# Kernel optimization log

Measured on AMD Instinct MI355X. Metric: run time of the kernel, lower is better.

The kernel has to match this reference:

```python
import jax, jax.numpy as jnp
import numpy as np

TOPK = 32
NUM_PT = 8192
NUM_KP = 8
HW = 19200


def _conv3(x, w, b):
    # x: [1, C, N], w: [O, C, 3] -> [1, O, N] (padding=1)
    y = jax.lax.conv_general_dilated(x, w, (1,), [(1, 1)],
                                     dimension_numbers=('NCH', 'OIH', 'NCH'))
    return y + b[None, :, None]


def setup_inputs() -> dict:
    key = jax.random.key(0)
    ks = jax.random.split(key, 64)

    def p(i, *shape):
        return (jax.random.normal(ks[i], shape, dtype=jnp.float32) * 0.05)

    inp = {
        'seg': jax.random.uniform(ks[0], (1, NUM_PT), dtype=jnp.float32),
        'img': jax.random.normal(ks[1], (1, 32, HW), dtype=jnp.float32),
        'cloud': jax.random.normal(ks[2], (1, NUM_PT, 3), dtype=jnp.float32),
        't': jax.random.normal(ks[3], (1, 3), dtype=jnp.float32),
        'choose': jax.random.randint(ks[4], (1, 1, NUM_PT), 0, HW),
        # Pseudo3DConv params (all 1x1 conv1d == channel matmul)
        'pconv1_w': p(5, 64, 3),    'pconv1_b': p(6, 64),
        'pconv2_w': p(7, 128, 64),  'pconv2_b': p(8, 128),
        'conv1_w': p(9, 64, 32),    'conv1_b': p(10, 64),
        'conv2_w': p(11, 128, 64),  'conv2_b': p(12, 128),
        'psconv1_w': p(13, 256, 128), 'psconv1_b': p(14, 256),
        'psconv2_w': p(15, 128, 256), 'psconv2_b': p(16, 128),
        'final_w': p(17, 128, 416), 'final_b': p(18, 128),
        # heads
        'seg1_w': p(19, 64, 128, 3), 'seg1_b': p(20, 64),
        'seg2_w': p(21, 32, 64),     'seg2_b': p(22, 32),
        'seg3_w': p(23, 1, 32),      'seg3_b': p(24, 1),
        'dis1_w': p(25, 64, 128, 3), 'dis1_b': p(26, 64),
        'dis2_w': p(27, 32, 64),     'dis2_b': p(28, 32),
        'dis3_w': p(29, 1, 32),      'dis3_b': p(30, 1),
        'lin1_w': p(31, 90, 128),    'lin1_b': p(32, 90),
        'lin2_w': p(33, 64, 90),     'lin2_b': p(34, 64),
        'lin3_w': p(35, 3 * NUM_KP, 64), 'lin3_b': p(36, 3 * NUM_KP),
    }
    return inp


def reference(seg, img, cloud, t, choose,
              pconv1_w, pconv1_b, pconv2_w, pconv2_b,
              conv1_w, conv1_b, conv2_w, conv2_b,
              psconv1_w, psconv1_b, psconv2_w, psconv2_b,
              final_w, final_b,
              seg1_w, seg1_b, seg2_w, seg2_b, seg3_w, seg3_b,
              dis1_w, dis1_b, dis2_w, dis2_b, dis3_w, dis3_b,
              lin1_w, lin1_b, lin2_w, lin2_b, lin3_w, lin3_b):
    lrelu = jax.nn.leaky_relu  # slope 0.01, same as torch default
    N = NUM_PT

    # gather per-point image features at chosen pixels: [N, 32]
    feat = jnp.take(img[0], choose[0, 0], axis=1).T
    c = cloud[0]  # [N, 3]

    # ---- KNN (self included, as in knn_cuda) ----
    d2 = jnp.sum((c[:, None, :] - c[None, :, :]) ** 2, axis=-1)  # [N, N]
    _, idx = jax.lax.top_k(-d2, TOPK)  # [N, K] nearest neighbors

    # ---- point-feature MLP (pconv1 -> lrelu -> pconv2) ----
    pf = lrelu(c @ pconv1_w.T + pconv1_b) @ pconv2_w.T + pconv2_b  # [N, 128]

    # ---- vectorized per-point neighbor gather + MLP + weighted maxpool ----
    nf = feat[idx]    # [N, K, 32]
    npf = pf[idx]     # [N, K, 128]
    npos = c[idx]     # [N, K, 3]
    w = jax.nn.softmax(-jnp.linalg.norm(c[:, None, :] - npos, axis=-1), axis=1)  # [N, K]

    f = lrelu(nf @ conv1_w.T + conv1_b) @ conv2_w.T + conv2_b          # [N, K, 128]
    fp = lrelu(npf @ psconv1_w.T + psconv1_b) @ psconv2_w.T + psconv2_b  # [N, K, 128]
    f = jnp.max(f * w[..., None], axis=1)    # [N, 128]
    fp = jnp.max(fp * w[..., None], axis=1)  # [N, 128]

    # final2 = [fp | img_feat], final1 = [f | cloud_feat] -> cat -> [N, 416]
    final = jnp.concatenate([fp, feat, f, pf], axis=1)
    fused = lrelu(final) @ final_w.T + final_b  # [N, 128]
    fused = fused.T[None]  # [1, 128, N]

    def pw(x, w_, b_):  # 1x1 conv1d on [1, C, N]
        return jnp.einsum('oc,bcn->bon', w_, x) + b_[None, :, None]

    # segmentation head
    h = lrelu(_conv3(fused, seg1_w, seg1_b))
    seg_pre = pw(lrelu(pw(h, seg2_w, seg2_b)), seg3_w, seg3_b).reshape(1, N)

    # distance-to-center weighting (norm along coord dim, softmax over points)
    dis_center = jax.nn.softmax(
        jnp.linalg.norm(cloud - (-t)[:, None, :], axis=2), axis=1)  # [1, N]

    # distance head (on unweighted fused features, matching torch op order)
    h = lrelu(_conv3(fused, dis1_w, dis1_b))
    dis_pre = pw(lrelu(pw(h, dis2_w, dis2_b)), dis3_w, dis3_b).reshape(1, N)

    # weight fused features by center distance and segmentation, sum-pool
    fused = fused * dis_center[:, None, :] * seg[:, None, :]
    g = jnp.sum(fused, axis=2)  # [1, 128]

    kp = lrelu(g @ lin1_w.T + lin1_b)
    kp = lrelu(kp @ lin2_w.T + lin2_b)
    keypoints = (kp @ lin3_w.T + lin3_b).reshape(1, NUM_KP, 3)
    return keypoints, dis_pre, dis_center, seg_pre
```

## Files before the change

### kernel.cpp

```cpp
#include <hip/hip_runtime.h>
#include <math.h>

#define NPT 8192
#define HWIMG 19200
#define KCAP 128

using short8 = __attribute__((ext_vector_type(8))) short;
using short4v = __attribute__((ext_vector_type(4))) short;
using f32x4  = __attribute__((ext_vector_type(4))) float;

__device__ __forceinline__ float lrelu(float x) { return x > 0.f ? x : 0.01f * x; }
__device__ __forceinline__ unsigned short f2bf(float v) {
  unsigned u = __float_as_uint(v);
  return (unsigned short)((u + 0x7fffu + ((u >> 16) & 1u)) >> 16);
}
__device__ __forceinline__ float bf2f(unsigned short h) {
  return __uint_as_float(((unsigned)h) << 16);
}
__device__ __forceinline__ void split2(float v, unsigned short& h, unsigned short& l) {
  h = f2bf(v);
  l = f2bf(v - bf2f(h));
}
__device__ __forceinline__ void mfma3(f32x4& acc, short8 ah, short8 al, short8 wh, short8 wl) {
  acc = __builtin_amdgcn_mfma_f32_16x16x32_bf16(ah, wh, acc, 0, 0, 0);
  acc = __builtin_amdgcn_mfma_f32_16x16x32_bf16(al, wh, acc, 0, 0, 0);
  acc = __builtin_amdgcn_mfma_f32_16x16x32_bf16(ah, wl, acc, 0, 0, 0);
}

__device__ __forceinline__ int swz(int o, int k, int Kc) {
  return ((((o >> 4) * Kc + (k >> 5)) << 6) + (((k >> 3) & 3) << 4) + (o & 15)) * 8 + (k & 7);
}

#define OFF_PCONV2  0
#define OFF_CONV1   8192
#define OFF_CONV2   10240
#define OFF_PSCONV1 18432
#define OFF_PSCONV2 51200
#define OFF_FINAL   83968
#define OFF_W3      137216
#define OFF_W2P     186368

#define S_C4    NPT
#define S_G     129
#define S_BIASC 128
#define S_B2C   64
#define S_FEAT  (NPT*32)
#define S_W3    49152
#define S_W2P   8192
#define S_WSPL  OFF_W3
#define PREP_TOTAL (S_C4 + S_G + S_BIASC + S_B2C + S_FEAT + S_W3 + S_W2P + S_WSPL)
__global__ void k_prep(const float* __restrict__ cloud, const int* __restrict__ choose,
                       const float* __restrict__ img,
                       const float* __restrict__ seg1_w, const float* __restrict__ dis1_w,
                       const float* __restrict__ seg1_b, const float* __restrict__ dis1_b,
                       const float* __restrict__ seg2_w, const float* __restrict__ dis2_w,
                       const float* __restrict__ seg2_b, const float* __restrict__ dis2_b,
                       const float* __restrict__ pconv2_w, const float* __restrict__ conv1_w,
                       const float* __restrict__ conv2_w, const float* __restrict__ psconv1_w,
                       const float* __restrict__ psconv2_w, const float* __restrict__ final_w,
                       float* __restrict__ c4, float* __restrict__ g,
                       float* __restrict__ biasc, float* __restrict__ bias2c,
                       float* __restrict__ feat,
                       unsigned short* __restrict__ feat_h, unsigned short* __restrict__ feat_l,
                       unsigned short* __restrict__ Wh, unsigned short* __restrict__ Wl) {
  int j = blockIdx.x * blockDim.x + threadIdx.x;
  if (j < S_C4) {
    float x = cloud[j*3+0], y = cloud[j*3+1], z = cloud[j*3+2];
    float4 v; v.x = x; v.y = y; v.z = z; v.w = x*x + y*y + z*z;
    ((float4*)c4)[j] = v;
    return;
  }
  j -= S_C4;
  if (j < S_G) { g[j] = 0.f; return; }
  j -= S_G;
  if (j < S_BIASC) { biasc[j] = (j < 64) ? seg1_b[j] : dis1_b[j-64]; return; }
  j -= S_BIASC;
  if (j < S_B2C) { bias2c[j] = (j < 32) ? seg2_b[j] : dis2_b[j-32]; return; }
  j -= S_B2C;
  if (j < S_FEAT) {
    int n = j >> 5, ch = j & 31;
    float v = img[ch*HWIMG + choose[n]];
    feat[j] = v;
    unsigned short hh, ll; split2(v, hh, ll);
    int d = swz(n, ch, 1);
    feat_h[d] = hh; feat_l[d] = ll;
    return;
  }
  j -= S_FEAT;
  if (j < S_W3) {
    int h = j / 24576, r = j - h*24576, o = r / 384, k = r - o*384;
    int t = k >> 7, c = k & 127;
    float v = (h ? dis1_w : seg1_w)[o*384 + c*3 + t];
    unsigned short hh, ll; split2(v, hh, ll);
    int d = OFF_W3 + swz(h*64 + o, k, 12);
    Wh[d] = hh; Wl[d] = ll;
    return;
  }
  j -= S_W3;
  if (j < S_W2P) {
    int o = j >> 7, c = j & 127;
    float v = 0.f;
    if (o < 32) { if (c < 64) v = seg2_w[o*64 + c]; }
    else        { if (c >= 64) v = dis2_w[(o-32)*64 + (c-64)]; }
    unsigned short hh, ll; split2(v, hh, ll);
    int d = OFF_W2P + swz(o, c, 4);
    Wh[d] = hh; Wl[d] = ll;
    return;
  }
  j -= S_W2P;
  if (j < S_WSPL) {
    float v; int d;
    if (j < OFF_CONV1) {
      int o = j >> 6, k = j & 63;
      v = pconv2_w[j]; d = OFF_PCONV2 + swz(o, k, 2);
    } else if (j < OFF_CONV2) {
      int jj = j - OFF_CONV1, o = jj >> 5, k = jj & 31;
      v = conv1_w[jj]; d = OFF_CONV1 + swz(o, k, 1);
    } else if (j < OFF_PSCONV1) {
      int jj = j - OFF_CONV2, o = jj >> 6, k = jj & 63;
      v = conv2_w[jj]; d = OFF_CONV2 + swz(o, k, 2);
    } else if (j < OFF_PSCONV2) {
      int jj = j - OFF_PSCONV1, o = jj >> 7, k = jj & 127;
      v = psconv1_w[jj]; d = OFF_PSCONV1 + swz(o, k, 4);
    } else if (j < OFF_FINAL) {
      int jj = j - OFF_PSCONV2, o = jj >> 8, k = jj & 255;
      v = psconv2_w[jj]; d = OFF_PSCONV2 + swz(o, k, 8);
    } else {
      int jj = j - OFF_FINAL, o = jj / 416, k = jj - o*416;
      v = final_w[jj]; d = OFF_FINAL + swz(o, k, 13);
    }
    unsigned short hh, ll; split2(v, hh, ll);
    Wh[d] = hh; Wl[d] = ll;
  }
}

__device__ __forceinline__ unsigned bsort32u(unsigned key, int lane) {
#pragma unroll
  for (int k = 2; k <= 64; k <<= 1) {
#pragma unroll
    for (int j = k >> 1; j > 0; j >>= 1) {
      unsigned o = __shfl_xor(key, j, 64);
      bool keepmin = (((lane & j) == 0) == ((lane & k) == 0));
      key = ((o < key) == keepmin) ? o : key;
    }
  }
  return key;
}
__device__ __forceinline__ unsigned long long bsort64(unsigned long long key, int lane) {
#pragma unroll
  for (int k = 2; k <= 64; k <<= 1) {
#pragma unroll
    for (int j = k >> 1; j > 0; j >>= 1) {
      unsigned long long o = __shfl_xor(key, j, 64);
      bool keepmin = (((lane & j) == 0) == ((lane & k) == 0));
      bool omin = o < key;
      key = (omin == keepmin) ? o : key;
    }
  }
  return key;
}
__device__ __forceinline__ unsigned long long bmerge64(unsigned long long key, int lane) {
#pragma unroll
  for (int j = 32; j > 0; j >>= 1) {
    unsigned long long o = __shfl_xor(key, j, 64);
    bool keepmin = ((lane & j) == 0);
    bool omin = o < key;
    key = (omin == keepmin) ? o : key;
  }
  return key;
}

#define MEGA_GRID 3073
__global__ __launch_bounds__(256) void k_mega(const float4* __restrict__ c4,
                                              int* __restrict__ idxo, float* __restrict__ wo,
                                              const float* __restrict__ cloud,
                                              const float* __restrict__ tvec,
                                              float* __restrict__ dc,
                                              const float* __restrict__ pconv1_w, const float* __restrict__ pconv1_b,
                                              const float* __restrict__ pconv2_b, const float* __restrict__ psconv1_b,
                                              const float* __restrict__ psconv2_b,
                                              const unsigned short* __restrict__ feat_h,
                                              const unsigned short* __restrict__ feat_l,
                                              const float* __restrict__ conv1_b, const float* __restrict__ conv2_b,
                                              const unsigned short* __restrict__ Wh,
                                              const unsigned short* __restrict__ Wl,
                                              float* __restrict__ pf, float* __restrict__ Yfp,
                                              float* __restrict__ Yf) {
  __shared__ __align__(16) char smem[16384];
  int tid = threadIdx.x, lane = tid & 63, w = tid >> 6;
  int mr = lane & 15, q = lane >> 4;
  if (blockIdx.x > 2048) {
    unsigned short* sh_h = (unsigned short*)smem;
    unsigned short* sh_l = (unsigned short*)(smem + 8192);
    int cb = blockIdx.x - 2049;
    if (cb < 512) {
      int m0 = cb * 16;
      float4 cp = c4[m0 + mr];
      short8 ah0, al0, ah1, al1;
#pragma unroll
      for (int j = 0; j < 8; ++j) {
        int c0 = q*8 + j, c1 = 32 + q*8 + j;
        float v0 = lrelu(fmaf(cp.x, pconv1_w[c0*3+0], fmaf(cp.y, pconv1_w[c0*3+1],
                          fmaf(cp.z, pconv1_w[c0*3+2], pconv1_b[c0]))));
        float v1 = lrelu(fmaf(cp.x, pconv1_w[c1*3+0], fmaf(cp.y, pconv1_w[c1*3+1],
                          fmaf(cp.z, pconv1_w[c1*3+2], pconv1_b[c1]))));
        unsigned short hh, ll;
        split2(v0, hh, ll); ah0[j] = (short)hh; al0[j] = (short)ll;
        split2(v1, hh, ll); ah1[j] = (short)hh; al1[j] = (short)ll;
      }
      f32x4 acc[2];
#pragma unroll
      for (int t = 0; t < 2; ++t) { f32x4 z = {0.f,0.f,0.f,0.f}; acc[t] = z; }
      const unsigned short* W2h = Wh + OFF_PCONV2;
      const unsigned short* W2l = Wl + OFF_PCONV2;
#pragma unroll
      for (int tt = 0; tt < 2; ++tt) {
        int t1 = 2*w + tt;
        int w0 = ((t1*2 + 0)*64 + lane)*8, w1 = ((t1*2 + 1)*64 + lane)*8;
        mfma3(acc[tt], ah0, al0, *(const short8*)(W2h + w0), *(const short8*)(W2l + w0));
        mfma3(acc[tt], ah1, al1, *(const short8*)(W2h + w1), *(const short8*)(W2l + w1));
      }
#pragma unroll
      for (int tt = 0; tt < 2; ++tt) {
        int t1 = 2*w + tt, n = t1*16 + mr;
        float b = pconv2_b[n];
        int ks2 = t1 >> 1, q2 = (t1 & 1)*2 + (mr >> 3), jd = mr & 7;
#pragma unroll
        for (int r = 0; r < 4; ++r) {
          int row = q*4 + r;
          float v = acc[tt][r] + b;
          pf[(size_t)(m0+row)*128 + n] = v;
          unsigned short hh, ll; split2(v, hh, ll);
          int p = ((ks2*16 + row)*4 + q2)*8 + jd;
          sh_h[p] = hh; sh_l[p] = ll;
        }
      }
      __syncthreads();
      f32x4 acc3[2];
#pragma unroll
      for (int t = 0; t < 2; ++t) { f32x4 z = {0.f,0.f,0.f,0.f}; acc3[t] = z; }
      const unsigned short* W3h = Wh + OFF_PSCONV1;
      const unsigned short* W3l = Wl + OFF_PSCONV1;
      const unsigned short* W4h = Wh + OFF_PSCONV2;
      const unsigned short* W4l = Wl + OFF_PSCONV2;
#pragma unroll
      for (int h = 0; h < 2; ++h) {
        f32x4 acc2[2];
#pragma unroll
        for (int t = 0; t < 2; ++t) { f32x4 z = {0.f,0.f,0.f,0.f}; acc2[t] = z; }
#pragma unroll
        for (int ks = 0; ks < 4; ++ks) {
          int ap = ((ks*16 + mr)*4 + q)*8;
          short8 ah = *(const short8*)&sh_h[ap];
          short8 al = *(const short8*)&sh_l[ap];
#pragma unroll
          for (int tt = 0; tt < 2; ++tt) {
            int ts = h*8 + 2*w + tt;
            int wb = ((ts*4 + ks)*64 + lane)*8;
            mfma3(acc2[tt], ah, al, *(const short8*)(W3h + wb), *(const short8*)(W3l + wb));
          }
        }
#pragma unroll
        for (int tt = 0; tt < 2; ++tt) {
          int tl = 2*w + tt;
          int n = h*128 + tl*16 + mr;
          float b = psconv1_b[n];
          int ks3 = tl >> 1, q3 = (tl & 1)*2 + (mr >> 3), jd = mr & 7;
#pragma unroll
          for (int r = 0; r < 4; ++r) {
            int row = q*4 + r;
            float v = lrelu(acc2[tt][r] + b);
            unsigned short hh, ll; split2(v, hh, ll);
            int p = 2048 + ((ks3*16 + row)*4 + q3)*8 + jd;
            sh_h[p] = hh; sh_l[p] = ll;
          }
        }
        __syncthreads();
#pragma unroll
        for (int ks = 0; ks < 4; ++ks) {
          int ap = 2048 + ((ks*16 + mr)*4 + q)*8;
          short8 ah = *(const short8*)&sh_h[ap];
          short8 al = *(const short8*)&sh_l[ap];
#pragma unroll
          for (int tt = 0; tt < 2; ++tt) {
            int wb = (((2*w+tt)*8 + h*4 + ks)*64 + lane)*8;
            mfma3(acc3[tt], ah, al, *(const short8*)(W4h + wb), *(const short8*)(W4l + wb));
          }
        }
        __syncthreads();
      }
#pragma unroll
      for (int tt = 0; tt < 2; ++tt) {
        int n = (2*w+tt)*16 + mr;
        float b = psconv2_b[n];
#pragma unroll
        for (int r = 0; r < 4; ++r)
          Yfp[(size_t)(m0 + q*4 + r)*128 + n] = acc3[tt][r] + b;
      }
    } else {
      int m0 = (cb - 512) * 16;
      int ab = ((m0 >> 4)*64 + lane)*8;
      short8 ah = *(const short8*)(feat_h + ab);
      short8 al = *(const short8*)(feat_l + ab);
      f32x4 acc = {0.f,0.f,0.f,0.f};
      const unsigned short* W1h = Wh + OFF_CONV1;
      const unsigned short* W1l = Wl + OFF_CONV1;
      {
        int wb = (w*64 + lane)*8;
        mfma3(acc, ah, al, *(const short8*)(W1h + wb), *(const short8*)(W1l + wb));
      }
      {
        int n = w*16 + mr;
        float b = conv1_b[n];
        int ks2 = n >> 5, q2 = (n >> 3) & 3, jd = mr & 7;
#pragma unroll
        for (int r = 0; r < 4; ++r) {
          int row = q*4 + r;
          float v = lrelu(acc[r] + b);
          unsigned short hh, ll; split2(v, hh, ll);
          int p = ((ks2*16 + row)*4 + q2)*8 + jd;
          sh_h[p] = hh; sh_l[p] = ll;
        }
      }
      __syncthreads();
      f32x4 acc2[2];
#pragma unroll
      for (int t = 0; t < 2; ++t) { f32x4 z = {0.f,0.f,0.f,0.f}; acc2[t] = z; }
      const unsigned short* W2h = Wh + OFF_CONV2;
      const unsigned short* W2l = Wl + OFF_CONV2;
#pragma unroll
      for (int ks = 0; ks < 2; ++ks) {
        int ap = ((ks*16 + mr)*4 + q)*8;
        short8 a2 = *(const short8*)&sh_h[ap];
        short8 a2l = *(const short8*)&sh_l[ap];
#pragma unroll
        for (int tt = 0; tt < 2; ++tt) {
          int wb = (((2*w+tt)*2 + ks)*64 + lane)*8;
          mfma3(acc2[tt], a2, a2l, *(const short8*)(W2h + wb), *(const short8*)(W2l + wb));
        }
      }
#pragma unroll
      for (int tt = 0; tt < 2; ++tt) {
        int n = (2*w+tt)*16 + mr;
        float b = conv2_b[n];
#pragma unroll
        for (int r = 0; r < 4; ++r)
          Yf[(size_t)(m0 + q*4 + r)*128 + n] = acc2[tt][r] + b;
      }
    }
    return;
  }
  if (blockIdx.x == 2048) {
    float* sred = (float*)smem;
    float tx = tvec[0], ty = tvec[1], tz = tvec[2];
    float v[32];
    float m = -INFINITY;
#pragma unroll
    for (int i2 = 0; i2 < 32; ++i2) {
      int n = i2*256 + tid;
      float ax = cloud[n*3+0] + tx, ay = cloud[n*3+1] + ty, az = cloud[n*3+2] + tz;
      v[i2] = sqrtf(ax*ax + ay*ay + az*az);
      m = fmaxf(m, v[i2]);
    }
#pragma unroll
    for (int o = 1; o < 64; o <<= 1) m = fmaxf(m, __shfl_xor(m, o, 64));
    if (lane == 0) sred[w] = m;
    __syncthreads();
    m = fmaxf(fmaxf(sred[0], sred[1]), fmaxf(sred[2], sred[3]));
    __syncthreads();
    float s = 0.f;
#pragma unroll
    for (int i2 = 0; i2 < 32; ++i2) { v[i2] = expf(v[i2] - m); s += v[i2]; }
#pragma unroll
    for (int o = 1; o < 64; o <<= 1) s += __shfl_xor(s, o, 64);
    if (lane == 0) sred[w] = s;
    __syncthreads();
    s = sred[0] + sred[1] + sred[2] + sred[3];
#pragma unroll
    for (int i2 = 0; i2 < 32; ++i2) dc[i2*256 + tid] = v[i2] / s;
    return;
  }
  float (*smin)[256] = (float(*)[256])smem;
  float* sTv = (float*)(smem + 4096);
  int*   scnt = (int*)(smem + 4112);
  float (*sd)[KCAP] = (float(*)[KCAP])(smem + 4128);
  int   (*sj)[KCAP] = (int(*)[KCAP])(smem + 6176);
  int q0 = blockIdx.x * 4;
  float4 p0 = c4[q0], p1 = c4[q0+1], p2 = c4[q0+2], p3 = c4[q0+3];
  float p0x = -2.f*p0.x, p0y = -2.f*p0.y, p0z = -2.f*p0.z;
  float p1x = -2.f*p1.x, p1y = -2.f*p1.y, p1z = -2.f*p1.z;
  float p2x = -2.f*p2.x, p2y = -2.f*p2.y, p2z = -2.f*p2.z;
  float p3x = -2.f*p3.x, p3y = -2.f*p3.y, p3z = -2.f*p3.z;
#define DDOT(PX,PY,PZ,PW,CJ) fmaf(PX,(CJ).x, fmaf(PY,(CJ).y, fmaf(PZ,(CJ).z, PW + (CJ).w)))
  float m0 = INFINITY, m1 = INFINITY, m2 = INFINITY, m3 = INFINITY;
  for (int t = 0; t < 32; ++t) {
    float4 cj = c4[t*256 + tid];
    m0 = fminf(m0, DDOT(p0x,p0y,p0z,p0.w,cj));
    m1 = fminf(m1, DDOT(p1x,p1y,p1z,p1.w,cj));
    m2 = fminf(m2, DDOT(p2x,p2y,p2z,p2.w,cj));
    m3 = fminf(m3, DDOT(p3x,p3y,p3z,p3.w,cj));
  }
  smin[0][tid] = m0; smin[1][tid] = m1; smin[2][tid] = m2; smin[3][tid] = m3;
  if (tid < 4) scnt[tid] = 0;
  __syncthreads();
  {
    float4 vv = *(const float4*)&smin[w][lane*4];
    float m4 = fmaxf(fminf(fminf(vv.x, vv.y), fminf(vv.z, vv.w)), 0.f);
    unsigned key = bsort32u(__float_as_uint(m4), lane);
    float T = __uint_as_float(__shfl(key, 31, 64));
    if (lane == 0) sTv[w] = T * (1.f + 2e-5f) + 4e-5f;
  }
  __syncthreads();
  float T0 = sTv[0], T1 = sTv[1], T2 = sTv[2], T3 = sTv[3];
  for (int t = 0; t < 32; ++t) {
    int j = t*256 + tid;
    float4 cj = c4[j];
    float d;
#define APPEND(Q, P) { \
    float dx_ = (P).x-cj.x, dy_ = (P).y-cj.y, dz_ = (P).z-cj.z; \
    float de_ = dx_*dx_ + dy_*dy_ + dz_*dz_; \
    int p_ = atomicAdd(&scnt[Q],1); if (p_ < KCAP) { sd[Q][p_] = de_; sj[Q][p_] = j; } }
    d = DDOT(p0x,p0y,p0z,p0.w,cj); if (d <= T0) APPEND(0, p0);
    d = DDOT(p1x,p1y,p1z,p1.w,cj); if (d <= T1) APPEND(1, p1);
    d = DDOT(p2x,p2y,p2z,p2.w,cj); if (d <= T2) APPEND(2, p2);
    d = DDOT(p3x,p3y,p3z,p3.w,cj); if (d <= T3) APPEND(3, p3);
  }
  __syncthreads();
  int M = scnt[w]; if (M > KCAP) M = KCAP;
  unsigned long long key = (lane < M)
      ? (((unsigned long long)__float_as_uint(sd[w][lane]) << 32) | (unsigned)sj[w][lane])
      : ~0ull;
  key = bsort64(key, lane);
  for (int base = 64; base < M; base += 64) {
    unsigned long long nk = (base + lane < M)
        ? (((unsigned long long)__float_as_uint(sd[w][base+lane]) << 32) | (unsigned)sj[w][base+lane])
        : ~0ull;
    nk = bsort64(nk, lane);
    nk = __shfl_xor(nk, 63, 64);
    key = key < nk ? key : nk;
    key = bmerge64(key, lane);
  }
  float dsel = __uint_as_float((unsigned)(key >> 32));
  int   jsel = (int)(unsigned)(key & 0xffffffffu);
  float v = -sqrtf(dsel);
  float mx = v;
#pragma unroll
  for (int o = 1; o < 32; o <<= 1) mx = fmaxf(mx, __shfl_xor(mx, o, 64));
  float e = expf(v - mx);
  float s = e;
#pragma unroll
  for (int o = 1; o < 32; o <<= 1) s += __shfl_xor(s, o, 64);
  if (lane < 32) {
    int qd = q0 + w;
    wo[qd*32 + lane] = e / s;
    idxo[qd*32 + lane] = jsel;
  }
}

__global__ __launch_bounds__(256) void k_tail(const float* __restrict__ Yf,
                                              const float* __restrict__ Yfp,
                                              const float* __restrict__ feat,
                                              const float* __restrict__ pf,
                                              const int* __restrict__ idx,
                                              const float* __restrict__ wsm,
                                              const unsigned short* __restrict__ Wh,
                                              const unsigned short* __restrict__ Wl,
                                              const float* __restrict__ final_b,
                                              const float* __restrict__ biasc,
                                              const float* __restrict__ bias2c,
                                              const float* __restrict__ segw, const float* __restrict__ segb,
                                              const float* __restrict__ disw, const float* __restrict__ disb,
                                              unsigned short* __restrict__ fusedh,
                                              unsigned short* __restrict__ fusedl,
                                              float* __restrict__ osegp, float* __restrict__ odisp) {
  __shared__ int sjn[18][32];
  __shared__ float swn[18][32];
  __shared__ __align__(16) char sbuf[37440];
  int tid = threadIdx.x, lane = tid & 63, w = tid >> 6;
  int mr = lane & 15, q = lane >> 4;
  int mt = blockIdx.x, m0 = mt * 16;
  for (int t = tid; t < 18*32; t += 256) {
    int lr = t >> 5, k = t & 31, gr = m0 - 1 + lr;
    if (gr >= 0 && gr < NPT) { sjn[lr][k] = idx[gr*32+k]; swn[lr][k] = wsm[gr*32+k]; }
    else { sjn[lr][k] = 0; swn[lr][k] = 0.f; }
  }
  __syncthreads();
  for (int t = tid; t < 1872; t += 256) {
    int lr, col;
    float4 v4;
    if (t < 1152) {
      lr = t >> 6; int arr = (t >> 5) & 1, cg = t & 31;
      const float* Y = arr ? Yf : Yfp;
      float ax = -INFINITY, ay = -INFINITY, az = -INFINITY, aw = -INFINITY;
#pragma unroll 8
      for (int k = 0; k < 32; ++k) {
        float4 vv = *(const float4*)&Y[(size_t)sjn[lr][k]*128 + cg*4];
        float wk = swn[lr][k];
        ax = fmaxf(ax, wk*vv.x); ay = fmaxf(ay, wk*vv.y);
        az = fmaxf(az, wk*vv.z); aw = fmaxf(aw, wk*vv.w);
      }
      v4.x = lrelu(ax); v4.y = lrelu(ay); v4.z = lrelu(az); v4.w = lrelu(aw);
      col = (arr ? 160 : 0) + cg*4;
    } else if (t < 1728) {
      int u = t - 1152; lr = u >> 5; int cg = u & 31;
      int gr = m0 - 1 + lr;
      int gc = gr < 0 ? 0 : (gr >= NPT ? NPT-1 : gr);
      float4 p4 = *(const float4*)&pf[(size_t)gc*128 + cg*4];
      v4.x = lrelu(p4.x); v4.y = lrelu(p4.y); v4.z = lrelu(p4.z); v4.w = lrelu(p4.w);
      col = 288 + cg*4;
    } else {
      int u = t - 1728; lr = u >> 3; int cg = u & 7;
      int gr = m0 - 1 + lr;
      int gc = gr < 0 ? 0 : (gr >= NPT ? NPT-1 : gr);
      float4 p4 = *(const float4*)&feat[(size_t)gc*32 + cg*4];
      v4.x = lrelu(p4.x); v4.y = lrelu(p4.y); v4.z = lrelu(p4.z); v4.w = lrelu(p4.w);
      col = 128 + cg*4;
    }
    int gr = m0 - 1 + lr;
    if (gr < 0 || gr >= NPT) { v4.x = 0.f; v4.y = 0.f; v4.z = 0.f; v4.w = 0.f; }
    int ks = col >> 5, qq = (col >> 3) & 3, j0 = col & 7;
    char* base = sbuf + (ks*18 + lr)*80 + qq*16 + j0*2;
    short4v hv, lv;
    unsigned short hh, ll;
    split2(v4.x, hh, ll); hv[0] = (short)hh; lv[0] = (short)ll;
    split2(v4.y, hh, ll); hv[1] = (short)hh; lv[1] = (short)ll;
    split2(v4.z, hh, ll); hv[2] = (short)hh; lv[2] = (short)ll;
    split2(v4.w, hh, ll); hv[3] = (short)hh; lv[3] = (short)ll;
    *(short4v*)base = hv;
    *(short4v*)(base + 18720) = lv;
  }
  __syncthreads();
  f32x4 accA[2], accB[2];
#pragma unroll
  for (int t = 0; t < 2; ++t) {
    f32x4 z = {0.f,0.f,0.f,0.f}; accA[t] = z; accB[t] = z;
  }
  const unsigned short* WFh = Wh + OFF_FINAL;
  const unsigned short* WFl = Wl + OFF_FINAL;
#pragma unroll
  for (int ks = 0; ks < 13; ++ks) {
    int arB = 16 + mr; if (arB > 17) arB = 17;
    const char* pA = sbuf + (ks*18 + mr)*80 + q*16;
    const char* pB = sbuf + (ks*18 + arB)*80 + q*16;
    short8 ahA = *(const short8*)pA;
    short8 alA = *(const short8*)(pA + 18720);
    short8 ahB = *(const short8*)pB;
    short8 alB = *(const short8*)(pB + 18720);
#pragma unroll
    for (int tt = 0; tt < 2; ++tt) {
      int wb = (((2*w+tt)*13 + ks)*64 + lane)*8;
      short8 wh = *(const short8*)(WFh + wb);
      short8 wl = *(const short8*)(WFl + wb);
      mfma3(accA[tt], ahA, alA, wh, wl);
      mfma3(accB[tt], ahB, alB, wh, wl);
    }
  }
  __syncthreads();
#pragma unroll
  for (int tile = 0; tile < 2; ++tile) {
#pragma unroll
    for (int tt = 0; tt < 2; ++tt) {
      int t2 = 2*w + tt, n = t2*16 + mr;
      float b = final_b[n];
      int ksA = t2 >> 1, qq = (t2 & 1)*2 + (mr >> 3), jd = mr & 7;
#pragma unroll
      for (int r = 0; r < 4; ++r) {
        int lr = tile*16 + q*4 + r;
        if (lr > 17) continue;
        int gr = m0 - 1 + lr;
        float v = (tile ? accB[tt][r] : accA[tt][r]) + b;
        if (gr < 0 || gr >= NPT) v = 0.f;
        unsigned short hh, ll; split2(v, hh, ll);
        char* p = sbuf + (ksA*18 + lr)*80 + qq*16 + jd*2;
        *(unsigned short*)p = hh;
        *(unsigned short*)(p + 5760) = ll;
      }
    }
  }
  __syncthreads();
  {
    int ks2 = tid >> 6, q2 = (tid >> 4) & 3, mr2 = tid & 15;
    int lr = mr2 + 1;
    const char* p = sbuf + (ks2*18 + lr)*80 + q2*16;
    short8 oh = *(const short8*)p;
    short8 ol = *(const short8*)(p + 5760);
    size_t pos = ((size_t)mt*256 + tid)*8;
    *(short8*)(fusedh + pos) = oh;
    *(short8*)(fusedl + pos) = ol;
  }
  f32x4 acc3[2];
#pragma unroll
  for (int t = 0; t < 2; ++t) { f32x4 z = {0.f,0.f,0.f,0.f}; acc3[t] = z; }
  const unsigned short* W3h = Wh + OFF_W3;
  const unsigned short* W3l = Wl + OFF_W3;
#pragma unroll
  for (int ks = 0; ks < 12; ++ks) {
    int tap = ks >> 2, ksA = ks & 3;
    int ar = mr + tap;
    const char* p = sbuf + (ksA*18 + ar)*80 + q*16;
    short8 ah = *(const short8*)p;
    short8 al = *(const short8*)(p + 5760);
#pragma unroll
    for (int tt = 0; tt < 2; ++tt) {
      int wb = (((2*w+tt)*12 + ks)*64 + lane)*8;
      mfma3(acc3[tt], ah, al, *(const short8*)(W3h + wb), *(const short8*)(W3l + wb));
    }
  }
#pragma unroll
  for (int tt = 0; tt < 2; ++tt) {
    int t2 = 2*w + tt, n = t2*16 + mr;
    float b = biasc[n];
    int ks2 = t2 >> 1, q2 = (t2 & 1)*2 + (mr >> 3), jd = mr & 7;
#pragma unroll
    for (int r = 0; r < 4; ++r) {
      int row = q*4 + r;
      float v = lrelu(acc3[tt][r] + b);
      unsigned short hh, ll; split2(v, hh, ll);
      char* p = sbuf + 11520 + (ks2*16 + row)*80 + q2*16 + jd*2;
      *(unsigned short*)p = hh;
      *(unsigned short*)(p + 5120) = ll;
    }
  }
  __syncthreads();
  f32x4 acc4 = {0.f,0.f,0.f,0.f};
  const unsigned short* WPh = Wh + OFF_W2P;
  const unsigned short* WPl = Wl + OFF_W2P;
#pragma unroll
  for (int ks = 0; ks < 4; ++ks) {
    const char* p = sbuf + 11520 + (ks*16 + mr)*80 + q*16;
    short8 ah = *(const short8*)p;
    short8 al = *(const short8*)(p + 5120);
    int wb = ((w*4 + ks)*64 + lane)*8;
    mfma3(acc4, ah, al, *(const short8*)(WPh + wb), *(const short8*)(WPl + wb));
  }
  float hw = (w < 2) ? segw[w*16 + mr] : disw[(w-2)*16 + mr];
  float bb = bias2c[w*16 + mr];
  float* shead = (float*)(sbuf + 21760);
#pragma unroll
  for (int r = 0; r < 4; ++r)
    shead[(w*16 + q*4 + r)*17 + mr] = lrelu(acc4[r] + bb) * hw;
  __syncthreads();
  if (tid < 16) {
    float a = 0.f;
#pragma unroll
    for (int i = 0; i < 16; ++i) a += shead[(tid)*17 + i] + shead[(16 + tid)*17 + i];
    osegp[m0 + tid] = a + segb[0];
  } else if (tid < 32) {
    int r2 = tid - 16;
    float a = 0.f;
#pragma unroll
    for (int i = 0; i < 16; ++i) a += shead[(32 + r2)*17 + i] + shead[(48 + r2)*17 + i];
    odisp[m0 + r2] = a + disb[0];
  }
}

__global__ __launch_bounds__(256) void k_gk(const unsigned short* __restrict__ Ah,
                                            const unsigned short* __restrict__ Al,
                                            const float* __restrict__ dc,
                                            const float* __restrict__ seg,
                                            float* __restrict__ g,
                                            const float* __restrict__ l1w, const float* __restrict__ l1b,
                                            const float* __restrict__ l2w, const float* __restrict__ l2b,
                                            const float* __restrict__ l3w, const float* __restrict__ l3b,
                                            float* __restrict__ o_kp) {
  __shared__ float sred[2048];
  __shared__ int slast;
  int tid = threadIdx.x;
  int b = blockIdx.x;
  float pg[8] = {0.f,0.f,0.f,0.f,0.f,0.f,0.f,0.f};
  int mrr = tid & 15;
  for (int mi = 0; mi < 16; ++mi) {
    int m = b*16 + mi;
    int row = m*16 + mrr;
    float wrow = dc[row] * seg[row];
    size_t pos = ((size_t)m*256 + tid)*8;
    short8 hv = *(const short8*)(Ah + pos);
    short8 lv = *(const short8*)(Al + pos);
#pragma unroll
    for (int j = 0; j < 8; ++j)
      pg[j] += (bf2f((unsigned short)hv[j]) + bf2f((unsigned short)lv[j])) * wrow;
  }
#pragma unroll
  for (int j = 0; j < 8; ++j) sred[tid*8 + j] = pg[j];
  __syncthreads();
  if (tid < 128) {
    int ks = tid >> 5, q2 = (tid >> 3) & 3, j = tid & 7;
    float s = 0.f;
#pragma unroll
    for (int mr2 = 0; mr2 < 16; ++mr2) s += sred[((ks<<6) + (q2<<4) + mr2)*8 + j];
    atomicAdd(&g[tid], s);
  }
  __threadfence();
  __syncthreads();
  if (tid == 0) slast = (atomicAdd((int*)(g + 128), 1) == 31);
  __syncthreads();
  if (!slast) return;
  __shared__ float sg[128], s1[90], s2[64];
  if (tid < 128) sg[tid] = atomicAdd(&g[tid], 0.f);
  __syncthreads();
  if (tid < 90) {
    float a = l1b[tid];
    for (int i = 0; i < 128; ++i) a += sg[i]*l1w[tid*128+i];
    s1[tid] = lrelu(a);
  }
  __syncthreads();
  if (tid < 64) {
    float a = l2b[tid];
    for (int i = 0; i < 90; ++i) a += s1[i]*l2w[tid*90+i];
    s2[tid] = lrelu(a);
  }
  __syncthreads();
  if (tid < 24) {
    float a = l3b[tid];
    for (int i = 0; i < 64; ++i) a += s2[i]*l3w[tid*64+i];
    o_kp[tid] = a;
  }
}

extern "C" void kernel_launch(void* const* d_in, const int* in_sizes, int n_in,
                              void* d_out, int out_size, void* d_ws, size_t ws_size,
                              hipStream_t stream) {
  const float* seg      = (const float*)d_in[0];
  const float* img      = (const float*)d_in[1];
  const float* cloud    = (const float*)d_in[2];
  const float* tvec     = (const float*)d_in[3];
  const int*   choose   = (const int*)d_in[4];
  const float* pconv1_w = (const float*)d_in[5];
  const float* pconv1_b = (const float*)d_in[6];
  const float* pconv2_w = (const float*)d_in[7];
  const float* pconv2_b = (const float*)d_in[8];
  const float* conv1_w  = (const float*)d_in[9];
  const float* conv1_b  = (const float*)d_in[10];
  const float* conv2_w  = (const float*)d_in[11];
  const float* conv2_b  = (const float*)d_in[12];
  const float* psconv1_w= (const float*)d_in[13];
  const float* psconv1_b= (const float*)d_in[14];
  const float* psconv2_w= (const float*)d_in[15];
  const float* psconv2_b= (const float*)d_in[16];
  const float* final_w  = (const float*)d_in[17];
  const float* final_b  = (const float*)d_in[18];
  const float* seg1_w   = (const float*)d_in[19];
  const float* seg1_b   = (const float*)d_in[20];
  const float* seg2_w   = (const float*)d_in[21];
  const float* seg2_b   = (const float*)d_in[22];
  const float* seg3_w   = (const float*)d_in[23];
  const float* seg3_b   = (const float*)d_in[24];
  const float* dis1_w   = (const float*)d_in[25];
  const float* dis1_b   = (const float*)d_in[26];
  const float* dis2_w   = (const float*)d_in[27];
  const float* dis2_b   = (const float*)d_in[28];
  const float* dis3_w   = (const float*)d_in[29];
  const float* dis3_b   = (const float*)d_in[30];
  const float* lin1_w   = (const float*)d_in[31];
  const float* lin1_b   = (const float*)d_in[32];
  const float* lin2_w   = (const float*)d_in[33];
  const float* lin2_b   = (const float*)d_in[34];
  const float* lin3_w   = (const float*)d_in[35];
  const float* lin3_b   = (const float*)d_in[36];

  float* out = (float*)d_out;
  float* ws  = (float*)d_ws;

  float* c4     = ws + 0;
  float* feat   = ws + 32768;
  unsigned short* feat_h = (unsigned short*)(ws + 294912);
  unsigned short* feat_l = (unsigned short*)(ws + 425984);
  float* pf     = ws + 557056;
  float* Yf     = ws + 1605632;
  float* Yfp    = ws + 2654208;
  int*   idx    = (int*)(ws + 3702784);
  float* wsm    = ws + 3964928;
  unsigned short* fusedh = (unsigned short*)(ws + 8683520);
  unsigned short* fusedl = (unsigned short*)(ws + 9207808);
  unsigned short* Wh    = (unsigned short*)(ws + 9732096);
  unsigned short* Wl    = (unsigned short*)(ws + 9829376);
  float* biasc  = ws + 9926656;
  float* bias2c = ws + 9926784;
  float* g      = ws + 9926848;

  float* o_kp   = out;
  float* o_disp = out + 24;
  float* o_dc   = out + 8216;
  float* o_segp = out + 16408;

  k_prep<<<(PREP_TOTAL + 255)/256, 256, 0, stream>>>(
      cloud, choose, img, seg1_w, dis1_w, seg1_b, dis1_b,
      seg2_w, dis2_w, seg2_b, dis2_b,
      pconv2_w, conv1_w, conv2_w, psconv1_w, psconv2_w, final_w,
      c4, g, biasc, bias2c, feat, feat_h, feat_l, Wh, Wl);

  k_mega<<<MEGA_GRID, 256, 0, stream>>>(
      (const float4*)c4, idx, wsm, cloud, tvec, o_dc,
      pconv1_w, pconv1_b, pconv2_b, psconv1_b, psconv2_b,
      feat_h, feat_l, conv1_b, conv2_b, Wh, Wl, pf, Yfp, Yf);

  k_tail<<<512, 256, 0, stream>>>(
      Yf, Yfp, feat, pf, idx, wsm, Wh, Wl,
      final_b, biasc, bias2c, seg3_w, seg3_b, dis3_w, dis3_b,
      fusedh, fusedl, o_segp, o_disp);

  k_gk<<<32, 256, 0, stream>>>(fusedh, fusedl, o_dc, seg, g,
                               lin1_w, lin1_b, lin2_w, lin2_b, lin3_w, lin3_b, o_kp);

  (void)in_sizes; (void)n_in; (void)out_size; (void)ws_size;
}
```

Before: 230.0 us.

## Fuse all four kernels into one persistent cooperative kernel with grid syncs

Merges the prep, mega (knn/chain/softmax), tail and global-keypoint kernels into a single cooperative kernel. Blocks loop over virtual block indices, and grid.sync() separates the phases. This removes three kernel launches and their inter-kernel gaps. In exchange, the grid is capped by occupancy at up to 1024 blocks, so persistent blocks serialize work that used to be spread over thousands of blocks. Shared memory is now sized for the largest phase, which may limit occupancy, and each grid barrier has its own cost.

```diff
diff --git a/kernel.cpp b/kernel.cpp
--- a/kernel.cpp
+++ b/kernel.cpp
@@ -1,5 +1,8 @@
 #include <hip/hip_runtime.h>
+#include <hip/hip_cooperative_groups.h>
 #include <math.h>
+
+namespace cg = cooperative_groups;
 
 #define NPT 8192
 #define HWIMG 19200
@@ -26,7 +29,6 @@
   acc = __builtin_amdgcn_mfma_f32_16x16x32_bf16(al, wh, acc, 0, 0, 0);
   acc = __builtin_amdgcn_mfma_f32_16x16x32_bf16(ah, wl, acc, 0, 0, 0);
 }
-
 __device__ __forceinline__ int swz(int o, int k, int Kc) {
   return ((((o >> 4) * Kc + (k >> 5)) << 6) + (((k >> 3) & 3) << 4) + (o & 15)) * 8 + (k & 7);
 }
@@ -49,62 +51,101 @@
 #define S_W2P   8192
 #define S_WSPL  OFF_W3
 #define PREP_TOTAL (S_C4 + S_G + S_BIASC + S_B2C + S_FEAT + S_W3 + S_W2P + S_WSPL)
-__global__ void k_prep(const float* __restrict__ cloud, const int* __restrict__ choose,
-                       const float* __restrict__ img,
-                       const float* __restrict__ seg1_w, const float* __restrict__ dis1_w,
-                       const float* __restrict__ seg1_b, const float* __restrict__ dis1_b,
-                       const float* __restrict__ seg2_w, const float* __restrict__ dis2_w,
-                       const float* __restrict__ seg2_b, const float* __restrict__ dis2_b,
-                       const float* __restrict__ pconv2_w, const float* __restrict__ conv1_w,
-                       const float* __restrict__ conv2_w, const float* __restrict__ psconv1_w,
-                       const float* __restrict__ psconv2_w, const float* __restrict__ final_w,
-                       float* __restrict__ c4, float* __restrict__ g,
-                       float* __restrict__ biasc, float* __restrict__ bias2c,
-                       float* __restrict__ feat,
-                       unsigned short* __restrict__ feat_h, unsigned short* __restrict__ feat_l,
-                       unsigned short* __restrict__ Wh, unsigned short* __restrict__ Wl) {
-  int j = blockIdx.x * blockDim.x + threadIdx.x;
+
+struct Args {
+  const float *seg, *img, *cloud, *tvec;
+  const int* choose;
+  const float *pconv1_w, *pconv1_b, *pconv2_w, *pconv2_b;
+  const float *conv1_w, *conv1_b, *conv2_w, *conv2_b;
+  const float *psconv1_w, *psconv1_b, *psconv2_w, *psconv2_b;
+  const float *final_w, *final_b;
+  const float *seg1_w, *seg1_b, *seg2_w, *seg2_b, *seg3_w, *seg3_b;
+  const float *dis1_w, *dis1_b, *dis2_w, *dis2_b, *dis3_w, *dis3_b;
+  const float *lin1_w, *lin1_b, *lin2_w, *lin2_b, *lin3_w, *lin3_b;
+  float *c4, *g, *biasc, *bias2c, *feat, *pf, *Yf, *Yfp, *wsm;
+  int* idx;
+  unsigned short *feat_h, *feat_l, *fusedh, *fusedl, *Wh, *Wl;
+  float *o_kp, *o_disp, *o_dc, *o_segp;
+};
+
+__device__ __forceinline__ unsigned bsort32u(unsigned key, int lane) {
+#pragma unroll
+  for (int k = 2; k <= 64; k <<= 1) {
+#pragma unroll
+    for (int j = k >> 1; j > 0; j >>= 1) {
+      unsigned o = __shfl_xor(key, j, 64);
+      bool keepmin = (((lane & j) == 0) == ((lane & k) == 0));
+      key = ((o < key) == keepmin) ? o : key;
+    }
+  }
+  return key;
+}
+__device__ __forceinline__ unsigned long long bsort64(unsigned long long key, int lane) {
+#pragma unroll
+  for (int k = 2; k <= 64; k <<= 1) {
+#pragma unroll
+    for (int j = k >> 1; j > 0; j >>= 1) {
+      unsigned long long o = __shfl_xor(key, j, 64);
+      bool keepmin = (((lane & j) == 0) == ((lane & k) == 0));
+      bool omin = o < key;
+      key = (omin == keepmin) ? o : key;
+    }
+  }
+  return key;
+}
+__device__ __forceinline__ unsigned long long bmerge64(unsigned long long key, int lane) {
+#pragma unroll
+  for (int j = 32; j > 0; j >>= 1) {
+    unsigned long long o = __shfl_xor(key, j, 64);
+    bool keepmin = ((lane & j) == 0);
+    bool omin = o < key;
+    key = (omin == keepmin) ? o : key;
+  }
+  return key;
+}
+
+__device__ void prep_item(const Args& a, int j) {
   if (j < S_C4) {
-    float x = cloud[j*3+0], y = cloud[j*3+1], z = cloud[j*3+2];
+    float x = a.cloud[j*3+0], y = a.cloud[j*3+1], z = a.cloud[j*3+2];
     float4 v; v.x = x; v.y = y; v.z = z; v.w = x*x + y*y + z*z;
-    ((float4*)c4)[j] = v;
+    ((float4*)a.c4)[j] = v;
     return;
   }
   j -= S_C4;
-  if (j < S_G) { g[j] = 0.f; return; }
+  if (j < S_G) { a.g[j] = 0.f; return; }
   j -= S_G;
-  if (j < S_BIASC) { biasc[j] = (j < 64) ? seg1_b[j] : dis1_b[j-64]; return; }
+  if (j < S_BIASC) { a.biasc[j] = (j < 64) ? a.seg1_b[j] : a.dis1_b[j-64]; return; }
   j -= S_BIASC;
-  if (j < S_B2C) { bias2c[j] = (j < 32) ? seg2_b[j] : dis2_b[j-32]; return; }
+  if (j < S_B2C) { a.bias2c[j] = (j < 32) ? a.seg2_b[j] : a.dis2_b[j-32]; return; }
   j -= S_B2C;
   if (j < S_FEAT) {
     int n = j >> 5, ch = j & 31;
-    float v = img[ch*HWIMG + choose[n]];
-    feat[j] = v;
+    float v = a.img[ch*HWIMG + a.choose[n]];
+    a.feat[j] = v;
     unsigned short hh, ll; split2(v, hh, ll);
     int d = swz(n, ch, 1);
-    feat_h[d] = hh; feat_l[d] = ll;
+    a.feat_h[d] = hh; a.feat_l[d] = ll;
     return;
   }
   j -= S_FEAT;
   if (j < S_W3) {
     int h = j / 24576, r = j - h*24576, o = r / 384, k = r - o*384;
     int t = k >> 7, c = k & 127;
-    float v = (h ? dis1_w : seg1_w)[o*384 + c*3 + t];
+    float v = (h ? a.dis1_w : a.seg1_w)[o*384 + c*3 + t];
     unsigned short hh, ll; split2(v, hh, ll);
     int d = OFF_W3 + swz(h*64 + o, k, 12);
-    Wh[d] = hh; Wl[d] = ll;
+    a.Wh[d] = hh; a.Wl[d] = ll;
     return;
   }
   j -= S_W3;
   if (j < S_W2P) {
     int o = j >> 7, c = j & 127;
     float v = 0.f;
-    if (o < 32) { if (c < 64) v = seg2_w[o*64 + c]; }
-    else        { if (c >= 64) v = dis2_w[(o-32)*64 + (c-64)]; }
+    if (o < 32) { if (c < 64) v = a.seg2_w[o*64 + c]; }
+    else        { if (c >= 64) v = a.dis2_w[(o-32)*64 + (c-64)]; }
     unsigned short hh, ll; split2(v, hh, ll);
     int d = OFF_W2P + swz(o, c, 4);
-    Wh[d] = hh; Wl[d] = ll;
+    a.Wh[d] = hh; a.Wl[d] = ll;
     return;
   }
   j -= S_W2P;
@@ -112,280 +153,68 @@
     float v; int d;
     if (j < OFF_CONV1) {
       int o = j >> 6, k = j & 63;
-      v = pconv2_w[j]; d = OFF_PCONV2 + swz(o, k, 2);
+      v = a.pconv2_w[j]; d = OFF_PCONV2 + swz(o, k, 2);
     } else if (j < OFF_CONV2) {
       int jj = j - OFF_CONV1, o = jj >> 5, k = jj & 31;
-      v = conv1_w[jj]; d = OFF_CONV1 + swz(o, k, 1);
+      v = a.conv1_w[jj]; d = OFF_CONV1 + swz(o, k, 1);
     } else if (j < OFF_PSCONV1) {
       int jj = j - OFF_CONV2, o = jj >> 6, k = jj & 63;
-      v = conv2_w[jj]; d = OFF_CONV2 + swz(o, k, 2);
+      v = a.conv2_w[jj]; d = OFF_CONV2 + swz(o, k, 2);
     } else if (j < OFF_PSCONV2) {
       int jj = j - OFF_PSCONV1, o = jj >> 7, k = jj & 127;
-      v = psconv1_w[jj]; d = OFF_PSCONV1 + swz(o, k, 4);
+      v = a.psconv1_w[jj]; d = OFF_PSCONV1 + swz(o, k, 4);
     } else if (j < OFF_FINAL) {
       int jj = j - OFF_PSCONV2, o = jj >> 8, k = jj & 255;
-      v = psconv2_w[jj]; d = OFF_PSCONV2 + swz(o, k, 8);
+      v = a.psconv2_w[jj]; d = OFF_PSCONV2 + swz(o, k, 8);
     } else {
       int jj = j - OFF_FINAL, o = jj / 416, k = jj - o*416;
-      v = final_w[jj]; d = OFF_FINAL + swz(o, k, 13);
+      v = a.final_w[jj]; d = OFF_FINAL + swz(o, k, 13);
     }
     unsigned short hh, ll; split2(v, hh, ll);
-    Wh[d] = hh; Wl[d] = ll;
-  }
-}
-
-__device__ __forceinline__ unsigned bsort32u(unsigned key, int lane) {
-#pragma unroll
-  for (int k = 2; k <= 64; k <<= 1) {
-#pragma unroll
-    for (int j = k >> 1; j > 0; j >>= 1) {
-      unsigned o = __shfl_xor(key, j, 64);
-      bool keepmin = (((lane & j) == 0) == ((lane & k) == 0));
-      key = ((o < key) == keepmin) ? o : key;
-    }
-  }
-  return key;
-}
-__device__ __forceinline__ unsigned long long bsort64(unsigned long long key, int lane) {
-#pragma unroll
-  for (int k = 2; k <= 64; k <<= 1) {
-#pragma unroll
-    for (int j = k >> 1; j > 0; j >>= 1) {
-      unsigned long long o = __shfl_xor(key, j, 64);
-      bool keepmin = (((lane & j) == 0) == ((lane & k) == 0));
-      bool omin = o < key;
-      key = (omin == keepmin) ? o : key;
-    }
-  }
-  return key;
-}
-__device__ __forceinline__ unsigned long long bmerge64(unsigned long long key, int lane) {
-#pragma unroll
-  for (int j = 32; j > 0; j >>= 1) {
-    unsigned long long o = __shfl_xor(key, j, 64);
-    bool keepmin = ((lane & j) == 0);
-    bool omin = o < key;
-    key = (omin == keepmin) ? o : key;
-  }
-  return key;
-}
-
-#define MEGA_GRID 3073
-__global__ __launch_bounds__(256) void k_mega(const float4* __restrict__ c4,
-                                              int* __restrict__ idxo, float* __restrict__ wo,
-                                              const float* __restrict__ cloud,
-                                              const float* __restrict__ tvec,
-                                              float* __restrict__ dc,
-                                              const float* __restrict__ pconv1_w, const float* __restrict__ pconv1_b,
-                                              const float* __restrict__ pconv2_b, const float* __restrict__ psconv1_b,
-                                              const float* __restrict__ psconv2_b,
-                                              const unsigned short* __restrict__ feat_h,
-                                              const unsigned short* __restrict__ feat_l,
-                                              const float* __restrict__ conv1_b, const float* __restrict__ conv2_b,
-                                              const unsigned short* __restrict__ Wh,
-                                              const unsigned short* __restrict__ Wl,
-                                              float* __restrict__ pf, float* __restrict__ Yfp,
-                                              float* __restrict__ Yf) {
-  __shared__ __align__(16) char smem[16384];
-  int tid = threadIdx.x, lane = tid & 63, w = tid >> 6;
-  int mr = lane & 15, q = lane >> 4;
-  if (blockIdx.x > 2048) {
-    unsigned short* sh_h = (unsigned short*)smem;
-    unsigned short* sh_l = (unsigned short*)(smem + 8192);
-    int cb = blockIdx.x - 2049;
-    if (cb < 512) {
-      int m0 = cb * 16;
-      float4 cp = c4[m0 + mr];
-      short8 ah0, al0, ah1, al1;
-#pragma unroll
-      for (int j = 0; j < 8; ++j) {
-        int c0 = q*8 + j, c1 = 32 + q*8 + j;
-        float v0 = lrelu(fmaf(cp.x, pconv1_w[c0*3+0], fmaf(cp.y, pconv1_w[c0*3+1],
-                          fmaf(cp.z, pconv1_w[c0*3+2], pconv1_b[c0]))));
-        float v1 = lrelu(fmaf(cp.x, pconv1_w[c1*3+0], fmaf(cp.y, pconv1_w[c1*3+1],
-                          fmaf(cp.z, pconv1_w[c1*3+2], pconv1_b[c1]))));
-        unsigned short hh, ll;
-        split2(v0, hh, ll); ah0[j] = (short)hh; al0[j] = (short)ll;
-        split2(v1, hh, ll); ah1[j] = (short)hh; al1[j] = (short)ll;
-      }
-      f32x4 acc[2];
-#pragma unroll
-      for (int t = 0; t < 2; ++t) { f32x4 z = {0.f,0.f,0.f,0.f}; acc[t] = z; }
-      const unsigned short* W2h = Wh + OFF_PCONV2;
-      const unsigned short* W2l = Wl + OFF_PCONV2;
-#pragma unroll
-      for (int tt = 0; tt < 2; ++tt) {
-        int t1 = 2*w + tt;
-        int w0 = ((t1*2 + 0)*64 + lane)*8, w1 = ((t1*2 + 1)*64 + lane)*8;
-        mfma3(acc[tt], ah0, al0, *(const short8*)(W2h + w0), *(const short8*)(W2l + w0));
-        mfma3(acc[tt], ah1, al1, *(const short8*)(W2h + w1), *(const short8*)(W2l + w1));
-      }
-#pragma unroll
-      for (int tt = 0; tt < 2; ++tt) {
-        int t1 = 2*w + tt, n = t1*16 + mr;
-        float b = pconv2_b[n];
-        int ks2 = t1 >> 1, q2 = (t1 & 1)*2 + (mr >> 3), jd = mr & 7;
-#pragma unroll
-        for (int r = 0; r < 4; ++r) {
-          int row = q*4 + r;
-          float v = acc[tt][r] + b;
-          pf[(size_t)(m0+row)*128 + n] = v;
-          unsigned short hh, ll; split2(v, hh, ll);
-          int p = ((ks2*16 + row)*4 + q2)*8 + jd;
-          sh_h[p] = hh; sh_l[p] = ll;
-        }
-      }
-      __syncthreads();
-      f32x4 acc3[2];
-#pragma unroll
-      for (int t = 0; t < 2; ++t) { f32x4 z = {0.f,0.f,0.f,0.f}; acc3[t] = z; }
-      const unsigned short* W3h = Wh + OFF_PSCONV1;
-      const unsigned short* W3l = Wl + OFF_PSCONV1;
-      const unsigned short* W4h = Wh + OFF_PSCONV2;
-      const unsigned short* W4l = Wl + OFF_PSCONV2;
-#pragma unroll
-      for (int h = 0; h < 2; ++h) {
-        f32x4 acc2[2];
-#pragma unroll
-        for (int t = 0; t < 2; ++t) { f32x4 z = {0.f,0.f,0.f,0.f}; acc2[t] = z; }
-#pragma unroll
-        for (int ks = 0; ks < 4; ++ks) {
-          int ap = ((ks*16 + mr)*4 + q)*8;
-          short8 ah = *(const short8*)&sh_h[ap];
-          short8 al = *(const short8*)&sh_l[ap];
-#pragma unroll
-          for (int tt = 0; tt < 2; ++tt) {
-            int ts = h*8 + 2*w + tt;
-            int wb = ((ts*4 + ks)*64 + lane)*8;
-            mfma3(acc2[tt], ah, al, *(const short8*)(W3h + wb), *(const short8*)(W3l + wb));
-          }
-        }
-#pragma unroll
-        for (int tt = 0; tt < 2; ++tt) {
-          int tl = 2*w + tt;
-          int n = h*128 + tl*16 + mr;
-          float b = psconv1_b[n];
-          int ks3 = tl >> 1, q3 = (tl & 1)*2 + (mr >> 3), jd = mr & 7;
-#pragma unroll
-          for (int r = 0; r < 4; ++r) {
-            int row = q*4 + r;
-            float v = lrelu(acc2[tt][r] + b);
-            unsigned short hh, ll; split2(v, hh, ll);
-            int p = 2048 + ((ks3*16 + row)*4 + q3)*8 + jd;
-            sh_h[p] = hh; sh_l[p] = ll;
-          }
-        }
-        __syncthreads();
-#pragma unroll
-        for (int ks = 0; ks < 4; ++ks) {
-          int ap = 2048 + ((ks*16 + mr)*4 + q)*8;
-          short8 ah = *(const short8*)&sh_h[ap];
-          short8 al = *(const short8*)&sh_l[ap];
-#pragma unroll
-          for (int tt = 0; tt < 2; ++tt) {
-            int wb = (((2*w+tt)*8 + h*4 + ks)*64 + lane)*8;
-            mfma3(acc3[tt], ah, al, *(const short8*)(W4h + wb), *(const short8*)(W4l + wb));
-          }
-        }
-        __syncthreads();
-      }
-#pragma unroll
-      for (int tt = 0; tt < 2; ++tt) {
-        int n = (2*w+tt)*16 + mr;
-        float b = psconv2_b[n];
-#pragma unroll
-        for (int r = 0; r < 4; ++r)
-          Yfp[(size_t)(m0 + q*4 + r)*128 + n] = acc3[tt][r] + b;
-      }
-    } else {
-      int m0 = (cb - 512) * 16;
-      int ab = ((m0 >> 4)*64 + lane)*8;
-      short8 ah = *(const short8*)(feat_h + ab);
-      short8 al = *(const short8*)(feat_l + ab);
-      f32x4 acc = {0.f,0.f,0.f,0.f};
-      const unsigned short* W1h = Wh + OFF_CONV1;
-      const unsigned short* W1l = Wl + OFF_CONV1;
-      {
-        int wb = (w*64 + lane)*8;
-        mfma3(acc, ah, al, *(const short8*)(W1h + wb), *(const short8*)(W1l + wb));
-      }
-      {
-        int n = w*16 + mr;
-        float b = conv1_b[n];
-        int ks2 = n >> 5, q2 = (n >> 3) & 3, jd = mr & 7;
-#pragma unroll
-        for (int r = 0; r < 4; ++r) {
-          int row = q*4 + r;
-          float v = lrelu(acc[r] + b);
-          unsigned short hh, ll; split2(v, hh, ll);
-          int p = ((ks2*16 + row)*4 + q2)*8 + jd;
-          sh_h[p] = hh; sh_l[p] = ll;
-        }
-      }
-      __syncthreads();
-      f32x4 acc2[2];
-#pragma unroll
-      for (int t = 0; t < 2; ++t) { f32x4 z = {0.f,0.f,0.f,0.f}; acc2[t] = z; }
-      const unsigned short* W2h = Wh + OFF_CONV2;
-      const unsigned short* W2l = Wl + OFF_CONV2;
-#pragma unroll
-      for (int ks = 0; ks < 2; ++ks) {
-        int ap = ((ks*16 + mr)*4 + q)*8;
-        short8 a2 = *(const short8*)&sh_h[ap];
-        short8 a2l = *(const short8*)&sh_l[ap];
-#pragma unroll
-        for (int tt = 0; tt < 2; ++tt) {
-          int wb = (((2*w+tt)*2 + ks)*64 + lane)*8;
-          mfma3(acc2[tt], a2, a2l, *(const short8*)(W2h + wb), *(const short8*)(W2l + wb));
-        }
-      }
-#pragma unroll
-      for (int tt = 0; tt < 2; ++tt) {
-        int n = (2*w+tt)*16 + mr;
-        float b = conv2_b[n];
-#pragma unroll
-        for (int r = 0; r < 4; ++r)
-          Yf[(size_t)(m0 + q*4 + r)*128 + n] = acc2[tt][r] + b;
-      }
-    }
-    return;
-  }
-  if (blockIdx.x == 2048) {
-    float* sred = (float*)smem;
-    float tx = tvec[0], ty = tvec[1], tz = tvec[2];
-    float v[32];
-    float m = -INFINITY;
-#pragma unroll
-    for (int i2 = 0; i2 < 32; ++i2) {
-      int n = i2*256 + tid;
-      float ax = cloud[n*3+0] + tx, ay = cloud[n*3+1] + ty, az = cloud[n*3+2] + tz;
-      v[i2] = sqrtf(ax*ax + ay*ay + az*az);
-      m = fmaxf(m, v[i2]);
-    }
-#pragma unroll
-    for (int o = 1; o < 64; o <<= 1) m = fmaxf(m, __shfl_xor(m, o, 64));
-    if (lane == 0) sred[w] = m;
-    __syncthreads();
-    m = fmaxf(fmaxf(sred[0], sred[1]), fmaxf(sred[2], sred[3]));
-    __syncthreads();
-    float s = 0.f;
-#pragma unroll
-    for (int i2 = 0; i2 < 32; ++i2) { v[i2] = expf(v[i2] - m); s += v[i2]; }
-#pragma unroll
-    for (int o = 1; o < 64; o <<= 1) s += __shfl_xor(s, o, 64);
-    if (lane == 0) sred[w] = s;
-    __syncthreads();
-    s = sred[0] + sred[1] + sred[2] + sred[3];
-#pragma unroll
-    for (int i2 = 0; i2 < 32; ++i2) dc[i2*256 + tid] = v[i2] / s;
-    return;
-  }
+    a.Wh[d] = hh; a.Wl[d] = ll;
+  }
+}
+
+__device__ void dc_body(const Args& a, char* smem, int tid) {
+  float* sred = (float*)smem;
+  int lane = tid & 63, w = tid >> 6;
+  float tx = a.tvec[0], ty = a.tvec[1], tz = a.tvec[2];
+  float v[32];
+  float m = -INFINITY;
+#pragma unroll
+  for (int i2 = 0; i2 < 32; ++i2) {
+    int n = i2*256 + tid;
+    float ax = a.cloud[n*3+0] + tx, ay = a.cloud[n*3+1] + ty, az = a.cloud[n*3+2] + tz;
+    v[i2] = sqrtf(ax*ax + ay*ay + az*az);
+    m = fmaxf(m, v[i2]);
+  }
+#pragma unroll
+  for (int o = 1; o < 64; o <<= 1) m = fmaxf(m, __shfl_xor(m, o, 64));
+  if (lane == 0) sred[w] = m;
+  __syncthreads();
+  m = fmaxf(fmaxf(sred[0], sred[1]), fmaxf(sred[2], sred[3]));
+  __syncthreads();
+  float s = 0.f;
+#pragma unroll
+  for (int i2 = 0; i2 < 32; ++i2) { v[i2] = expf(v[i2] - m); s += v[i2]; }
+#pragma unroll
+  for (int o = 1; o < 64; o <<= 1) s += __shfl_xor(s, o, 64);
+  if (lane == 0) sred[w] = s;
+  __syncthreads();
+  s = sred[0] + sred[1] + sred[2] + sred[3];
+#pragma unroll
+  for (int i2 = 0; i2 < 32; ++i2) a.o_dc[i2*256 + tid] = v[i2] / s;
+}
+
+__device__ void knn_body(const Args& a, char* smem, int qb, int tid) {
   float (*smin)[256] = (float(*)[256])smem;
   float* sTv = (float*)(smem + 4096);
   int*   scnt = (int*)(smem + 4112);
   float (*sd)[KCAP] = (float(*)[KCAP])(smem + 4128);
   int   (*sj)[KCAP] = (int(*)[KCAP])(smem + 6176);
-  int q0 = blockIdx.x * 4;
+  int lane = tid & 63, w = tid >> 6;
+  const float4* c4 = (const float4*)a.c4;
+  int q0 = qb * 4;
   float4 p0 = c4[q0], p1 = c4[q0+1], p2 = c4[q0+2], p3 = c4[q0+3];
   float p0x = -2.f*p0.x, p0y = -2.f*p0.y, p0z = -2.f*p0.z;
   float p1x = -2.f*p1.x, p1y = -2.f*p1.y, p1z = -2.f*p1.z;
@@ -452,37 +281,185 @@
   for (int o = 1; o < 32; o <<= 1) s += __shfl_xor(s, o, 64);
   if (lane < 32) {
     int qd = q0 + w;
-    wo[qd*32 + lane] = e / s;
-    idxo[qd*32 + lane] = jsel;
-  }
-}
-
-__global__ __launch_bounds__(256) void k_tail(const float* __restrict__ Yf,
-                                              const float* __restrict__ Yfp,
-                                              const float* __restrict__ feat,
-                                              const float* __restrict__ pf,
-                                              const int* __restrict__ idx,
-                                              const float* __restrict__ wsm,
-                                              const unsigned short* __restrict__ Wh,
-                                              const unsigned short* __restrict__ Wl,
-                                              const float* __restrict__ final_b,
-                                              const float* __restrict__ biasc,
-                                              const float* __restrict__ bias2c,
-                                              const float* __restrict__ segw, const float* __restrict__ segb,
-                                              const float* __restrict__ disw, const float* __restrict__ disb,
-                                              unsigned short* __restrict__ fusedh,
-                                              unsigned short* __restrict__ fusedl,
-                                              float* __restrict__ osegp, float* __restrict__ odisp) {
-  __shared__ int sjn[18][32];
-  __shared__ float swn[18][32];
-  __shared__ __align__(16) char sbuf[37440];
-  int tid = threadIdx.x, lane = tid & 63, w = tid >> 6;
+    a.wsm[qd*32 + lane] = e / s;
+    a.idx[qd*32 + lane] = jsel;
+  }
+}
+
+__device__ void chain_body(const Args& a, char* smem, int cb, int tid) {
+  unsigned short* sh_h = (unsigned short*)smem;
+  unsigned short* sh_l = (unsigned short*)(smem + 8192);
+  int lane = tid & 63, w = tid >> 6;
   int mr = lane & 15, q = lane >> 4;
-  int mt = blockIdx.x, m0 = mt * 16;
+  const float4* c4 = (const float4*)a.c4;
+  if (cb < 512) {
+    int m0 = cb * 16;
+    float4 cp = c4[m0 + mr];
+    short8 ah0, al0, ah1, al1;
+#pragma unroll
+    for (int j = 0; j < 8; ++j) {
+      int c0 = q*8 + j, c1 = 32 + q*8 + j;
+      float v0 = lrelu(fmaf(cp.x, a.pconv1_w[c0*3+0], fmaf(cp.y, a.pconv1_w[c0*3+1],
+                        fmaf(cp.z, a.pconv1_w[c0*3+2], a.pconv1_b[c0]))));
+      float v1 = lrelu(fmaf(cp.x, a.pconv1_w[c1*3+0], fmaf(cp.y, a.pconv1_w[c1*3+1],
+                        fmaf(cp.z, a.pconv1_w[c1*3+2], a.pconv1_b[c1]))));
+      unsigned short hh, ll;
+      split2(v0, hh, ll); ah0[j] = (short)hh; al0[j] = (short)ll;
+      split2(v1, hh, ll); ah1[j] = (short)hh; al1[j] = (short)ll;
+    }
+    f32x4 acc[2];
+#pragma unroll
+    for (int t = 0; t < 2; ++t) { f32x4 z = {0.f,0.f,0.f,0.f}; acc[t] = z; }
+    const unsigned short* W2h = a.Wh + OFF_PCONV2;
+    const unsigned short* W2l = a.Wl + OFF_PCONV2;
+#pragma unroll
+    for (int tt = 0; tt < 2; ++tt) {
+      int t1 = 2*w + tt;
+      int w0 = ((t1*2 + 0)*64 + lane)*8, w1 = ((t1*2 + 1)*64 + lane)*8;
+      mfma3(acc[tt], ah0, al0, *(const short8*)(W2h + w0), *(const short8*)(W2l + w0));
+      mfma3(acc[tt], ah1, al1, *(const short8*)(W2h + w1), *(const short8*)(W2l + w1));
+    }
+#pragma unroll
+    for (int tt = 0; tt < 2; ++tt) {
+      int t1 = 2*w + tt, n = t1*16 + mr;
+      float b = a.pconv2_b[n];
+      int ks2 = t1 >> 1, q2 = (t1 & 1)*2 + (mr >> 3), jd = mr & 7;
+#pragma unroll
+      for (int r = 0; r < 4; ++r) {
+        int row = q*4 + r;
+        float v = acc[tt][r] + b;
+        a.pf[(size_t)(m0+row)*128 + n] = v;
+        unsigned short hh, ll; split2(v, hh, ll);
+        int p = ((ks2*16 + row)*4 + q2)*8 + jd;
+        sh_h[p] = hh; sh_l[p] = ll;
+      }
+    }
+    __syncthreads();
+    f32x4 acc3[2];
+#pragma unroll
+    for (int t = 0; t < 2; ++t) { f32x4 z = {0.f,0.f,0.f,0.f}; acc3[t] = z; }
+    const unsigned short* W3h = a.Wh + OFF_PSCONV1;
+    const unsigned short* W3l = a.Wl + OFF_PSCONV1;
+    const unsigned short* W4h = a.Wh + OFF_PSCONV2;
+    const unsigned short* W4l = a.Wl + OFF_PSCONV2;
+#pragma unroll
+    for (int h = 0; h < 2; ++h) {
+      f32x4 acc2[2];
+#pragma unroll
+      for (int t = 0; t < 2; ++t) { f32x4 z = {0.f,0.f,0.f,0.f}; acc2[t] = z; }
+#pragma unroll
+      for (int ks = 0; ks < 4; ++ks) {
+        int ap = ((ks*16 + mr)*4 + q)*8;
+        short8 ah = *(const short8*)&sh_h[ap];
+        short8 al = *(const short8*)&sh_l[ap];
+#pragma unroll
+        for (int tt = 0; tt < 2; ++tt) {
+          int ts = h*8 + 2*w + tt;
+          int wb = ((ts*4 + ks)*64 + lane)*8;
+          mfma3(acc2[tt], ah, al, *(const short8*)(W3h + wb), *(const short8*)(W3l + wb));
+        }
+      }
+#pragma unroll
+      for (int tt = 0; tt < 2; ++tt) {
+        int tl = 2*w + tt;
+        int n = h*128 + tl*16 + mr;
+        float b = a.psconv1_b[n];
+        int ks3 = tl >> 1, q3 = (tl & 1)*2 + (mr >> 3), jd = mr & 7;
+#pragma unroll
+        for (int r = 0; r < 4; ++r) {
+          int row = q*4 + r;
+          float v = lrelu(acc2[tt][r] + b);
+          unsigned short hh, ll; split2(v, hh, ll);
+          int p = 2048 + ((ks3*16 + row)*4 + q3)*8 + jd;
+          sh_h[p] = hh; sh_l[p] = ll;
+        }
+      }
+      __syncthreads();
+#pragma unroll
+      for (int ks = 0; ks < 4; ++ks) {
+        int ap = 2048 + ((ks*16 + mr)*4 + q)*8;
+        short8 ah = *(const short8*)&sh_h[ap];
+        short8 al = *(const short8*)&sh_l[ap];
+#pragma unroll
+        for (int tt = 0; tt < 2; ++tt) {
+          int wb = (((2*w+tt)*8 + h*4 + ks)*64 + lane)*8;
+          mfma3(acc3[tt], ah, al, *(const short8*)(W4h + wb), *(const short8*)(W4l + wb));
+        }
+      }
+      __syncthreads();
+    }
+#pragma unroll
+    for (int tt = 0; tt < 2; ++tt) {
+      int n = (2*w+tt)*16 + mr;
+      float b = a.psconv2_b[n];
+#pragma unroll
+      for (int r = 0; r < 4; ++r)
+        a.Yfp[(size_t)(m0 + q*4 + r)*128 + n] = acc3[tt][r] + b;
+    }
+  } else {
+    int m0 = (cb - 512) * 16;
+    int ab = ((m0 >> 4)*64 + lane)*8;
+    short8 ah = *(const short8*)(a.feat_h + ab);
+    short8 al = *(const short8*)(a.feat_l + ab);
+    f32x4 acc = {0.f,0.f,0.f,0.f};
+    const unsigned short* W1h = a.Wh + OFF_CONV1;
+    const unsigned short* W1l = a.Wl + OFF_CONV1;
+    {
+      int wb = (w*64 + lane)*8;
+      mfma3(acc, ah, al, *(const short8*)(W1h + wb), *(const short8*)(W1l + wb));
+    }
+    {
+      int n = w*16 + mr;
+      float b = a.conv1_b[n];
+      int ks2 = n >> 5, q2 = (n >> 3) & 3, jd = mr & 7;
+#pragma unroll
+      for (int r = 0; r < 4; ++r) {
+        int row = q*4 + r;
+        float v = lrelu(acc[r] + b);
+        unsigned short hh, ll; split2(v, hh, ll);
+        int p = ((ks2*16 + row)*4 + q2)*8 + jd;
+        sh_h[p] = hh; sh_l[p] = ll;
+      }
+    }
+    __syncthreads();
+    f32x4 acc2[2];
+#pragma unroll
+    for (int t = 0; t < 2; ++t) { f32x4 z = {0.f,0.f,0.f,0.f}; acc2[t] = z; }
+    const unsigned short* W2h = a.Wh + OFF_CONV2;
+    const unsigned short* W2l = a.Wl + OFF_CONV2;
+#pragma unroll
+    for (int ks = 0; ks < 2; ++ks) {
+      int ap = ((ks*16 + mr)*4 + q)*8;
+      short8 a2 = *(const short8*)&sh_h[ap];
+      short8 a2l = *(const short8*)&sh_l[ap];
+#pragma unroll
+      for (int tt = 0; tt < 2; ++tt) {
+        int wb = (((2*w+tt)*2 + ks)*64 + lane)*8;
+        mfma3(acc2[tt], a2, a2l, *(const short8*)(W2h + wb), *(const short8*)(W2l + wb));
+      }
+    }
+#pragma unroll
+    for (int tt = 0; tt < 2; ++tt) {
+      int n = (2*w+tt)*16 + mr;
+      float b = a.conv2_b[n];
+#pragma unroll
+      for (int r = 0; r < 4; ++r)
+        a.Yf[(size_t)(m0 + q*4 + r)*128 + n] = acc2[tt][r] + b;
+    }
+  }
+}
+
+__device__ void tail_body(const Args& a, char* smem, int mt, int tid) {
+  char* sbuf = smem;
+  short* sjn = (short*)(smem + 37440);
+  float* swn = (float*)(smem + 38592);
+  int lane = tid & 63, w = tid >> 6;
+  int mr = lane & 15, q = lane >> 4;
+  int m0 = mt * 16;
   for (int t = tid; t < 18*32; t += 256) {
     int lr = t >> 5, k = t & 31, gr = m0 - 1 + lr;
-    if (gr >= 0 && gr < NPT) { sjn[lr][k] = idx[gr*32+k]; swn[lr][k] = wsm[gr*32+k]; }
-    else { sjn[lr][k] = 0; swn[lr][k] = 0.f; }
+    if (gr >= 0 && gr < NPT) { sjn[lr*32+k] = (short)a.idx[gr*32+k]; swn[lr*32+k] = a.wsm[gr*32+k]; }
+    else { sjn[lr*32+k] = 0; swn[lr*32+k] = 0.f; }
   }
   __syncthreads();
   for (int t = tid; t < 1872; t += 256) {
@@ -490,12 +467,12 @@
     float4 v4;
     if (t < 1152) {
       lr = t >> 6; int arr = (t >> 5) & 1, cg = t & 31;
-      const float* Y = arr ? Yf : Yfp;
+      const float* Y = arr ? a.Yf : a.Yfp;
       float ax = -INFINITY, ay = -INFINITY, az = -INFINITY, aw = -INFINITY;
 #pragma unroll 8
       for (int k = 0; k < 32; ++k) {
-        float4 vv = *(const float4*)&Y[(size_t)sjn[lr][k]*128 + cg*4];
-        float wk = swn[lr][k];
+        float4 vv = *(const float4*)&Y[(size_t)sjn[lr*32+k]*128 + cg*4];
+        float wk = swn[lr*32+k];
         ax = fmaxf(ax, wk*vv.x); ay = fmaxf(ay, wk*vv.y);
         az = fmaxf(az, wk*vv.z); aw = fmaxf(aw, wk*vv.w);
       }
@@ -505,14 +482,14 @@
       int u = t - 1152; lr = u >> 5; int cg = u & 31;
       int gr = m0 - 1 + lr;
       int gc = gr < 0 ? 0 : (gr >= NPT ? NPT-1 : gr);
-      float4 p4 = *(const float4*)&pf[(size_t)gc*128 + cg*4];
+      float4 p4 = *(const float4*)&a.pf[(size_t)gc*128 + cg*4];
       v4.x = lrelu(p4.x); v4.y = lrelu(p4.y); v4.z = lrelu(p4.z); v4.w = lrelu(p4.w);
       col = 288 + cg*4;
     } else {
       int u = t - 1728; lr = u >> 3; int cg = u & 7;
       int gr = m0 - 1 + lr;
       int gc = gr < 0 ? 0 : (gr >= NPT ? NPT-1 : gr);
-      float4 p4 = *(const float4*)&feat[(size_t)gc*32 + cg*4];
+      float4 p4 = *(const float4*)&a.feat[(size_t)gc*32 + cg*4];
       v4.x = lrelu(p4.x); v4.y = lrelu(p4.y); v4.z = lrelu(p4.z); v4.w = lrelu(p4.w);
       col = 128 + cg*4;
     }
@@ -535,8 +512,8 @@
   for (int t = 0; t < 2; ++t) {
     f32x4 z = {0.f,0.f,0.f,0.f}; accA[t] = z; accB[t] = z;
   }
-  const unsigned short* WFh = Wh + OFF_FINAL;
-  const unsigned short* WFl = Wl + OFF_FINAL;
+  const unsigned short* WFh = a.Wh + OFF_FINAL;
+  const unsigned short* WFl = a.Wl + OFF_FINAL;
 #pragma unroll
   for (int ks = 0; ks < 13; ++ks) {
     int arB = 16 + mr; if (arB > 17) arB = 17;
@@ -561,7 +538,7 @@
 #pragma unroll
     for (int tt = 0; tt < 2; ++tt) {
       int t2 = 2*w + tt, n = t2*16 + mr;
-      float b = final_b[n];
+      float b = a.final_b[n];
       int ksA = t2 >> 1, qq = (t2 & 1)*2 + (mr >> 3), jd = mr & 7;
 #pragma unroll
       for (int r = 0; r < 4; ++r) {
@@ -585,14 +562,14 @@
     short8 oh = *(const short8*)p;
     short8 ol = *(const short8*)(p + 5760);
     size_t pos = ((size_t)mt*256 + tid)*8;
-    *(short8*)(fusedh + pos) = oh;
-    *(short8*)(fusedl + pos) = ol;
+    *(short8*)(a.fusedh + pos) = oh;
+    *(short8*)(a.fusedl + pos) = ol;
   }
   f32x4 acc3[2];
 #pragma unroll
   for (int t = 0; t < 2; ++t) { f32x4 z = {0.f,0.f,0.f,0.f}; acc3[t] = z; }
-  const unsigned short* W3h = Wh + OFF_W3;
-  const unsigned short* W3l = Wl + OFF_W3;
+  const unsigned short* W3h = a.Wh + OFF_W3;
+  const unsigned short* W3l = a.Wl + OFF_W3;
 #pragma unroll
   for (int ks = 0; ks < 12; ++ks) {
     int tap = ks >> 2, ksA = ks & 3;
@@ -609,7 +586,7 @@
 #pragma unroll
   for (int tt = 0; tt < 2; ++tt) {
     int t2 = 2*w + tt, n = t2*16 + mr;
-    float b = biasc[n];
+    float b = a.biasc[n];
     int ks2 = t2 >> 1, q2 = (t2 & 1)*2 + (mr >> 3), jd = mr & 7;
 #pragma unroll
     for (int r = 0; r < 4; ++r) {
@@ -623,8 +600,8 @@
   }
   __syncthreads();
   f32x4 acc4 = {0.f,0.f,0.f,0.f};
-  const unsigned short* WPh = Wh + OFF_W2P;
-  const unsigned short* WPl = Wl + OFF_W2P;
+  const unsigned short* WPh = a.Wh + OFF_W2P;
+  const unsigned short* WPl = a.Wl + OFF_W2P;
 #pragma unroll
   for (int ks = 0; ks < 4; ++ks) {
     const char* p = sbuf + 11520 + (ks*16 + mr)*80 + q*16;
@@ -633,49 +610,42 @@
     int wb = ((w*4 + ks)*64 + lane)*8;
     mfma3(acc4, ah, al, *(const short8*)(WPh + wb), *(const short8*)(WPl + wb));
   }
-  float hw = (w < 2) ? segw[w*16 + mr] : disw[(w-2)*16 + mr];
-  float bb = bias2c[w*16 + mr];
+  float hw = (w < 2) ? a.seg3_w[w*16 + mr] : a.dis3_w[(w-2)*16 + mr];
+  float bb = a.bias2c[w*16 + mr];
   float* shead = (float*)(sbuf + 21760);
 #pragma unroll
   for (int r = 0; r < 4; ++r)
     shead[(w*16 + q*4 + r)*17 + mr] = lrelu(acc4[r] + bb) * hw;
   __syncthreads();
   if (tid < 16) {
-    float a = 0.f;
-#pragma unroll
-    for (int i = 0; i < 16; ++i) a += shead[(tid)*17 + i] + shead[(16 + tid)*17 + i];
-    osegp[m0 + tid] = a + segb[0];
+    float s = 0.f;
+#pragma unroll
+    for (int i = 0; i < 16; ++i) s += shead[(tid)*17 + i] + shead[(16 + tid)*17 + i];
+    a.o_segp[m0 + tid] = s + a.seg3_b[0];
   } else if (tid < 32) {
     int r2 = tid - 16;
-    float a = 0.f;
-#pragma unroll
-    for (int i = 0; i < 16; ++i) a += shead[(32 + r2)*17 + i] + shead[(48 + r2)*17 + i];
-    odisp[m0 + r2] = a + disb[0];
-  }
-}
-
-__global__ __launch_bounds__(256) void k_gk(const unsigned short* __restrict__ Ah,
-                                            const unsigned short* __restrict__ Al,
-                                            const float* __restrict__ dc,
-                                            const float* __restrict__ seg,
-                                            float* __restrict__ g,
-                                            const float* __restrict__ l1w, const float* __restrict__ l1b,
-                                            const float* __restrict__ l2w, const float* __restrict__ l2b,
-                                            const float* __restrict__ l3w, const float* __restrict__ l3b,
-                                            float* __restrict__ o_kp) {
-  __shared__ float sred[2048];
-  __shared__ int slast;
-  int tid = threadIdx.x;
-  int b = blockIdx.x;
+    float s = 0.f;
+#pragma unroll
+    for (int i = 0; i < 16; ++i) s += shead[(32 + r2)*17 + i] + shead[(48 + r2)*17 + i];
+    a.o_disp[m0 + r2] = s + a.dis3_b[0];
+  }
+}
+
+__device__ void gk_body(const Args& a, char* smem, int b, int tid) {
+  float* sred = (float*)smem;
+  int* slast = (int*)(smem + 8192);
+  float* sg = (float*)(smem + 8208);
+  float* s1 = sg + 128;
+  float* s2 = s1 + 90;
   float pg[8] = {0.f,0.f,0.f,0.f,0.f,0.f,0.f,0.f};
   int mrr = tid & 15;
   for (int mi = 0; mi < 16; ++mi) {
     int m = b*16 + mi;
     int row = m*16 + mrr;
-    float wrow = dc[row] * seg[row];
+    float wrow = a.o_dc[row] * a.seg[row];
     size_t pos = ((size_t)m*256 + tid)*8;
-    short8 hv = *(const short8*)(Ah + pos);
-    short8 lv = *(const short8*)(Al + pos);
+    short8 hv = *(const short8*)(a.fusedh + pos);
+    short8 lv = *(const short8*)(a.fusedl + pos);
 #pragma unroll
     for (int j = 0; j < 8; ++j)
       pg[j] += (bf2f((unsigned short)hv[j]) + bf2f((unsigned short)lv[j])) * wrow;
@@ -688,119 +658,120 @@
     float s = 0.f;
 #pragma unroll
     for (int mr2 = 0; mr2 < 16; ++mr2) s += sred[((ks<<6) + (q2<<4) + mr2)*8 + j];
-    atomicAdd(&g[tid], s);
+    atomicAdd(&a.g[tid], s);
   }
   __threadfence();
   __syncthreads();
-  if (tid == 0) slast = (atomicAdd((int*)(g + 128), 1) == 31);
-  __syncthreads();
-  if (!slast) return;
-  __shared__ float sg[128], s1[90], s2[64];
-  if (tid < 128) sg[tid] = atomicAdd(&g[tid], 0.f);
+  if (tid == 0) *slast = (atomicAdd((int*)(a.g + 128), 1) == 31);
+  __syncthreads();
+  if (!*slast) return;
+  if (tid < 128) sg[tid] = atomicAdd(&a.g[tid], 0.f);
   __syncthreads();
   if (tid < 90) {
-    float a = l1b[tid];
-    for (int i = 0; i < 128; ++i) a += sg[i]*l1w[tid*128+i];
-    s1[tid] = lrelu(a);
+    float s = a.lin1_b[tid];
+    for (int i = 0; i < 128; ++i) s += sg[i]*a.lin1_w[tid*128+i];
+    s1[tid] = lrelu(s);
   }
   __syncthreads();
   if (tid < 64) {
-    float a = l2b[tid];
-    for (int i = 0; i < 90; ++i) a += s1[i]*l2w[tid*90+i];
-    s2[tid] = lrelu(a);
+    float s = a.lin2_b[tid];
+    for (int i = 0; i < 90; ++i) s += s1[i]*a.lin2_w[tid*90+i];
+    s2[tid] = lrelu(s);
   }
   __syncthreads();
   if (tid < 24) {
-    float a = l3b[tid];
-    for (int i = 0; i < 64; ++i) a += s2[i]*l3w[tid*64+i];
-    o_kp[tid] = a;
+    float s = a.lin3_b[tid];
+    for (int i = 0; i < 64; ++i) s += s2[i]*a.lin3_w[tid*64+i];
+    a.o_kp[tid] = s;
+  }
+}
+
+__global__ __launch_bounds__(256, 4) void k_all(Args a) {
+  __shared__ __align__(16) char smem[40896];
+  cg::grid_group grid = cg::this_grid();
+  int nb = gridDim.x, bid = blockIdx.x, tid = threadIdx.x;
+  if (bid == 0) {
+    dc_body(a, smem, tid);
+  } else {
+    for (int j = (bid-1)*256 + tid; j < PREP_TOTAL; j += (nb-1)*256) prep_item(a, j);
+  }
+  grid.sync();
+  for (int vb = bid; vb < 3072; vb += nb) {
+    __syncthreads();
+    if (vb < 2048) knn_body(a, smem, vb, tid);
+    else           chain_body(a, smem, vb - 2048, tid);
+  }
+  grid.sync();
+  for (int mt = bid; mt < 512; mt += nb) {
+    __syncthreads();
+    tail_body(a, smem, mt, tid);
+  }
+  grid.sync();
+  for (int vb = bid; vb < 32; vb += nb) {
+    __syncthreads();
+    gk_body(a, smem, vb, tid);
   }
 }
 
 extern "C" void kernel_launch(void* const* d_in, const int* in_sizes, int n_in,
                               void* d_out, int out_size, void* d_ws, size_t ws_size,
                               hipStream_t stream) {
-  const float* seg      = (const float*)d_in[0];
-  const float* img      = (const float*)d_in[1];
-  const float* cloud    = (const float*)d_in[2];
-  const float* tvec     = (const float*)d_in[3];
-  const int*   choose   = (const int*)d_in[4];
-  const float* pconv1_w = (const float*)d_in[5];
-  const float* pconv1_b = (const float*)d_in[6];
-  const float* pconv2_w = (const float*)d_in[7];
-  const float* pconv2_b = (const float*)d_in[8];
-  const float* conv1_w  = (const float*)d_in[9];
-  const float* conv1_b  = (const float*)d_in[10];
-  const float* conv2_w  = (const float*)d_in[11];
-  const float* conv2_b  = (const float*)d_in[12];
-  const float* psconv1_w= (const float*)d_in[13];
-  const float* psconv1_b= (const float*)d_in[14];
-  const float* psconv2_w= (const float*)d_in[15];
-  const float* psconv2_b= (const float*)d_in[16];
-  const float* final_w  = (const float*)d_in[17];
-  const float* final_b  = (const float*)d_in[18];
-  const float* seg1_w   = (const float*)d_in[19];
-  const float* seg1_b   = (const float*)d_in[20];
-  const float* seg2_w   = (const float*)d_in[21];
-  const float* seg2_b   = (const float*)d_in[22];
-  const float* seg3_w   = (const float*)d_in[23];
-  const float* seg3_b   = (const float*)d_in[24];
-  const float* dis1_w   = (const float*)d_in[25];
-  const float* dis1_b   = (const float*)d_in[26];
-  const float* dis2_w   = (const float*)d_in[27];
-  const float* dis2_b   = (const float*)d_in[28];
-  const float* dis3_w   = (const float*)d_in[29];
-  const float* dis3_b   = (const float*)d_in[30];
-  const float* lin1_w   = (const float*)d_in[31];
-  const float* lin1_b   = (const float*)d_in[32];
-  const float* lin2_w   = (const float*)d_in[33];
-  const float* lin2_b   = (const float*)d_in[34];
-  const float* lin3_w   = (const float*)d_in[35];
-  const float* lin3_b   = (const float*)d_in[36];
-
   float* out = (float*)d_out;
   float* ws  = (float*)d_ws;
 
-  float* c4     = ws + 0;
-  float* feat   = ws + 32768;
-  unsigned short* feat_h = (unsigned short*)(ws + 294912);
-  unsigned short* feat_l = (unsigned short*)(ws + 425984);
-  float* pf     = ws + 557056;
-  float* Yf     = ws + 1605632;
-  float* Yfp    = ws + 2654208;
-  int*   idx    = (int*)(ws + 3702784);
-  float* wsm    = ws + 3964928;
-  unsigned short* fusedh = (unsigned short*)(ws + 8683520);
-  unsigned short* fusedl = (unsigned short*)(ws + 9207808);
-  unsigned short* Wh    = (unsigned short*)(ws + 9732096);
-  unsigned short* Wl    = (unsigned short*)(ws + 9829376);
-  float* biasc  = ws + 9926656;
-  float* bias2c = ws + 9926784;
-  float* g      = ws + 9926848;
-
-  float* o_kp   = out;
-  float* o_disp = out + 24;
-  float* o_dc   = out + 8216;
-  float* o_segp = out + 16408;
-
-  k_prep<<<(PREP_TOTAL + 255)/256, 256, 0, stream>>>(
-      cloud, choose, img, seg1_w, dis1_w, seg1_b, dis1_b,
-      seg2_w, dis2_w, seg2_b, dis2_b,
-      pconv2_w, conv1_w, conv2_w, psconv1_w, psconv2_w, final_w,
-      c4, g, biasc, bias2c, feat, feat_h, feat_l, Wh, Wl);
-
-  k_mega<<<MEGA_GRID, 256, 0, stream>>>(
-      (const float4*)c4, idx, wsm, cloud, tvec, o_dc,
-      pconv1_w, pconv1_b, pconv2_b, psconv1_b, psconv2_b,
-      feat_h, feat_l, conv1_b, conv2_b, Wh, Wl, pf, Yfp, Yf);
-
-  k_tail<<<512, 256, 0, stream>>>(
-      Yf, Yfp, feat, pf, idx, wsm, Wh, Wl,
-      final_b, biasc, bias2c, seg3_w, seg3_b, dis3_w, dis3_b,
-      fusedh, fusedl, o_segp, o_disp);
-
-  k_gk<<<32, 256, 0, stream>>>(fusedh, fusedl, o_dc, seg, g,
-                               lin1_w, lin1_b, lin2_w, lin2_b, lin3_w, lin3_b, o_kp);
+  Args a;
+  a.seg      = (const float*)d_in[0];
+  a.img      = (const float*)d_in[1];
+  a.cloud    = (const float*)d_in[2];
+  a.tvec     = (const float*)d_in[3];
+  a.choose   = (const int*)d_in[4];
+  a.pconv1_w = (const float*)d_in[5];   a.pconv1_b = (const float*)d_in[6];
+  a.pconv2_w = (const float*)d_in[7];   a.pconv2_b = (const float*)d_in[8];
+  a.conv1_w  = (const float*)d_in[9];   a.conv1_b  = (const float*)d_in[10];
+  a.conv2_w  = (const float*)d_in[11];  a.conv2_b  = (const float*)d_in[12];
+  a.psconv1_w= (const float*)d_in[13];  a.psconv1_b= (const float*)d_in[14];
+  a.psconv2_w= (const float*)d_in[15];  a.psconv2_b= (const float*)d_in[16];
+  a.final_w  = (const float*)d_in[17];  a.final_b  = (const float*)d_in[18];
+  a.seg1_w   = (const float*)d_in[19];  a.seg1_b   = (const float*)d_in[20];
+  a.seg2_w   = (const float*)d_in[21];  a.seg2_b   = (const float*)d_in[22];
+  a.seg3_w   = (const float*)d_in[23];  a.seg3_b   = (const float*)d_in[24];
+  a.dis1_w   = (const float*)d_in[25];  a.dis1_b   = (const float*)d_in[26];
+  a.dis2_w   = (const float*)d_in[27];  a.dis2_b   = (const float*)d_in[28];
+  a.dis3_w   = (const float*)d_in[29];  a.dis3_b   = (const float*)d_in[30];
+  a.lin1_w   = (const float*)d_in[31];  a.lin1_b   = (const float*)d_in[32];
+  a.lin2_w   = (const float*)d_in[33];  a.lin2_b   = (const float*)d_in[34];
+  a.lin3_w   = (const float*)d_in[35];  a.lin3_b   = (const float*)d_in[36];
+
+  a.c4     = ws + 0;
+  a.feat   = ws + 32768;
+  a.feat_h = (unsigned short*)(ws + 294912);
+  a.feat_l = (unsigned short*)(ws + 425984);
+  a.pf     = ws + 557056;
+  a.Yf     = ws + 1605632;
+  a.Yfp    = ws + 2654208;
+  a.idx    = (int*)(ws + 3702784);
+  a.wsm    = ws + 3964928;
+  a.fusedh = (unsigned short*)(ws + 8683520);
+  a.fusedl = (unsigned short*)(ws + 9207808);
+  a.Wh     = (unsigned short*)(ws + 9732096);
+  a.Wl     = (unsigned short*)(ws + 9829376);
+  a.biasc  = ws + 9926656;
+  a.bias2c = ws + 9926784;
+  a.g      = ws + 9926848;
+
+  a.o_kp   = out;
+  a.o_disp = out + 24;
+  a.o_dc   = out + 8216;
+  a.o_segp = out + 16408;
+
+  int occ = 0;
+  hipOccupancyMaxActiveBlocksPerMultiprocessor(&occ, (const void*)k_all, 256, 0);
+  int grid = occ * 256;
+  if (grid > 1024) grid = 1024;
+  if (grid < 256) grid = 256;
+
+  void* params[] = { (void*)&a };
+  hipLaunchCooperativeKernel((const void*)k_all, dim3(grid), dim3(256), params, 0, stream);
 
   (void)in_sizes; (void)n_in; (void)out_size; (void)ws_size;
 }
```

Result: slower. 599.4 us (+160.6%).
